# Kernel tuning notes

Measured on AMD Instinct MI355X. Metric: run time of the kernel, lower is better.

The kernel has to match this reference:

```python
import jax, jax.numpy as jnp
import numpy as np

B, T, D = 2, 1024, 1024          # batch, seq, d_model
DI = 2 * D                        # ssm d_inner
N = 16                            # ssm state dim
H, HD = 16, 64                    # heads, head_dim
L = 256                           # MLA latent dim
E, K, F = 8, 2, 2048              # experts, top_k, d_ff
EPS = 1.1920929e-07               # torch RMSNorm default eps (float32 finfo eps)
AUX_COEF = 0.01


def rmsnorm(x, w):
    return x * jax.lax.rsqrt(jnp.mean(x * x, axis=-1, keepdims=True) + EPS) * w


def ternary_quantize(w):
    thresh = 0.5 * jnp.mean(jnp.abs(w))
    return (w > thresh).astype(w.dtype) - (w < -thresh).astype(w.dtype)


def ternary_ste(w):
    # forward uses quantized weights; backward is identity (STE)
    return w + jax.lax.stop_gradient(ternary_quantize(w) - w)


def setup_inputs():
    key = jax.random.key(0)
    ks = jax.random.split(key, 20)
    p = lambda k, s: jax.random.normal(k, s, jnp.float32) * 0.02
    return {
        'x': jax.random.normal(ks[0], (B, T, D), jnp.float32),
        'norm1_w': jnp.ones((D,), jnp.float32),
        'norm2_w': jnp.ones((D,), jnp.float32),
        'ssm_in_w': p(ks[1], (2 * DI, D)),
        'ssm_A_w': p(ks[2], (N, DI)),
        'ssm_B_w': p(ks[3], (N, DI)),
        'ssm_C_w': p(ks[4], (N, DI)),
        'ssm_norm_w': jnp.ones((DI,), jnp.float32),
        'ssm_out_w': p(ks[5], (D, DI)),
        'q_w': p(ks[6], (D, D)),
        'kv_down_w': p(ks[7], (L, D)),
        'k_up_w': p(ks[8], (D, L)),
        'v_up_w': p(ks[9], (D, L)),
        'attn_out_w': p(ks[10], (D, D)),
        'fuse_w': p(ks[11], (D, D)),
        'router_w': p(ks[12], (E, D)),
        'e_gate_w': p(ks[13], (E, F, D)),
        'e_up_w': p(ks[14], (E, F, D)),
        'e_down_w': p(ks[15], (E, D, F)),
        'e_gate_g': jnp.full((E,), 1.0 / np.sqrt(D), jnp.float32),
        'e_up_g': jnp.full((E,), 1.0 / np.sqrt(D), jnp.float32),
        'e_down_g': jnp.full((E,), 1.0 / np.sqrt(F), jnp.float32),
    }


def ssm_branch(h, ssm_in_w, ssm_A_w, ssm_B_w, ssm_C_w, ssm_norm_w, ssm_out_w):
    xz = jnp.einsum('btd,ed->bte', h, ssm_in_w)  # [B,T,2*DI]
    x_in = jax.nn.silu(xz[..., :DI]) * jax.nn.sigmoid(xz[..., DI:])  # [B,T,DI]
    A = -jnp.exp(jnp.clip(jnp.einsum('btd,nd->btn', x_in, ssm_A_w), -5.0, 0.0))
    Bs = jnp.einsum('btd,nd->btn', x_in, ssm_B_w)
    Cs = jnp.einsum('btd,nd->btn', x_in, ssm_C_w)

    def step(state, inp):  # state: [B, DI, N]
        xt, at, bt, ct = inp
        state = state * jnp.exp(at)[:, None, :] + xt[..., None] * bt[:, None, :]
        return state, jnp.sum(state * ct[:, None, :], axis=-1)

    init = jnp.zeros((B, DI, N), jnp.float32)
    xs = (x_in.transpose(1, 0, 2), A.transpose(1, 0, 2), Bs.transpose(1, 0, 2), Cs.transpose(1, 0, 2))
    _, ys = jax.lax.scan(step, init, xs)           # [T,B,DI]
    out = rmsnorm(ys.transpose(1, 0, 2), ssm_norm_w)
    return jnp.einsum('bti,di->btd', out, ssm_out_w)


def mla_attention(h, q_w, kv_down_w, k_up_w, v_up_w, attn_out_w):
    q = jnp.einsum('btd,ed->bte', h, q_w)
    lat = jnp.einsum('btd,ld->btl', h, kv_down_w)
    k = jnp.einsum('btl,dl->btd', lat, k_up_w)
    v = jnp.einsum('btl,dl->btd', lat, v_up_w)
    sh = lambda t: t.reshape(B, T, H, HD).transpose(0, 2, 1, 3)  # [B,H,T,HD]
    q, k, v = sh(q), sh(k), sh(v)
    scores = jnp.einsum('bhqd,bhkd->bhqk', q, k) * (HD ** -0.5)
    attn = jax.nn.softmax(scores, axis=-1)
    out = jnp.einsum('bhqk,bhkd->bhqd', attn, v)
    out = out.transpose(0, 2, 1, 3).reshape(B, T, D)
    return jnp.einsum('btd,ed->bte', out, attn_out_w)


def moe(xf, router_w, e_gate_w, e_up_w, e_down_w, e_gate_g, e_up_g, e_down_g):
    logits = jnp.einsum('td,ed->te', xf, router_w)
    probs = jax.nn.softmax(logits, axis=-1)
    topk_p, topk_i = jax.lax.top_k(probs, K)
    topk_w = topk_p / (jnp.sum(topk_p, axis=-1, keepdims=True) + 1e-09)
    # dense combine weights [tokens, E] (0 for non-selected experts -> same math)
    w_full = jnp.sum(jax.nn.one_hot(topk_i, E, dtype=xf.dtype) * topk_w[..., None], axis=1)
    g = jnp.einsum('td,efd->tef', xf, ternary_ste(e_gate_w)) * e_gate_g[None, :, None]
    u = jnp.einsum('td,efd->tef', xf, ternary_ste(e_up_w)) * e_up_g[None, :, None]
    hh = jax.nn.silu(g) * u
    y = jnp.einsum('tef,edf->ted', hh, ternary_ste(e_down_w)) * e_down_g[None, :, None]
    out = jnp.einsum('ted,te->td', y, w_full)
    mean_probs = jnp.mean(probs, axis=0)
    entropy = -jnp.sum(mean_probs * jnp.log(mean_probs + 1e-09))
    aux = -entropy * AUX_COEF
    return out, aux


def reference(x, norm1_w, norm2_w, ssm_in_w, ssm_A_w, ssm_B_w, ssm_C_w, ssm_norm_w, ssm_out_w,
              q_w, kv_down_w, k_up_w, v_up_w, attn_out_w, fuse_w, router_w,
              e_gate_w, e_up_w, e_down_w, e_gate_g, e_up_g, e_down_g):
    h = rmsnorm(x, norm1_w)
    ssm_out = ssm_branch(h, ssm_in_w, ssm_A_w, ssm_B_w, ssm_C_w, ssm_norm_w, ssm_out_w)
    attn_out = mla_attention(h, q_w, kv_down_w, k_up_w, v_up_w, attn_out_w)
    gate = jax.nn.sigmoid(jnp.einsum('btd,ed->bte', h, fuse_w))  # gated fusion
    x = x + gate * ssm_out + (1.0 - gate) * attn_out
    h2 = rmsnorm(x, norm2_w)
    moe_out, aux = moe(h2.reshape(-1, D), router_w, e_gate_w, e_up_w, e_down_w, e_gate_g, e_up_g, e_down_g)
    x = x + moe_out.reshape(B, T, D)
    return x, aux
```

## Files before the change

### kernel.cpp

```cpp
#include <hip/hip_runtime.h>

constexpr int kB = 2, kT = 1024, kD = 1024, kDI = 2048, kH = 16, kE = 8, kF = 2048;
constexpr int kBT = kB * kT;
constexpr float kEPS = 1.1920929e-07f;

constexpr size_t MF = 1024ull * 1024ull;
constexpr size_t F_H      = 0;
constexpr size_t F_HH     = 0;
constexpr size_t F_XIN    = 2*MF;
constexpr size_t F_EXPA   = 6*MF;
constexpr size_t F_CB     = 6*MF + 32768;
constexpr size_t F_CC     = 6*MF + 65536;
constexpr size_t F_P      = 7*MF;
constexpr size_t F_Q      = 8*MF;
constexpr size_t F_S0     = 9*MF;
constexpr size_t F_YS     = 10*MF;
constexpr size_t F_SSMO   = 14*MF;
constexpr size_t F_ATTNO  = 16*MF;
constexpr size_t F_H2     = 18*MF;
constexpr size_t F_NORMED = 20*MF;
constexpr size_t F_QB     = 20*MF;
constexpr size_t F_KB     = 22*MF;
constexpr size_t F_VB     = 24*MF;
constexpr size_t F_LAT    = 26*MF;
constexpr size_t F_CTX    = 26*MF + MF/2;
constexpr size_t F_FUSE   = 28*MF + MF/2;
constexpr size_t F_XZ     = 31*MF;
constexpr size_t F_SCORES = 31*MF;
constexpr size_t F_QG8    = 31*MF;
constexpr size_t F_QU8    = 35*MF;
constexpr size_t F_QD8    = 39*MF;
constexpr size_t F_MISC   = 47*MF;
constexpr size_t P_PART   = F_MISC;
constexpr size_t P_THRESH = F_MISC + 3072;
constexpr size_t P_PROBS  = F_MISC + 3080;
constexpr size_t I_COUNTS = F_MISC + 3088;
constexpr size_t I_OFFS   = F_MISC + 3096;
constexpr size_t I_CURSOR = F_MISC + 3105;
constexpr size_t I_NTILES = F_MISC + 3113;
constexpr size_t I_TILEE  = F_MISC + 3114;
constexpr size_t I_TILEB  = F_MISC + 3194;
constexpr size_t I_TOPI   = F_MISC + 3274;
constexpr size_t P_TOPW   = F_MISC + 7370;
constexpr size_t I_PAIRT  = F_MISC + 11466;
constexpr size_t P_PAIRW  = F_MISC + 19658;
constexpr size_t WS_FLOATS = F_MISC + 32768;

__device__ __forceinline__ float sigmoidf_(float v) { return 1.f / (1.f + expf(-v)); }

__global__ void zero_k(float* p, int n) {
    int i = blockIdx.x * blockDim.x + threadIdx.x;
    if (i < n) p[i] = 0.f;
}

__global__ __launch_bounds__(256) void rmsnorm_k(const float* __restrict__ x,
                                                 const float* __restrict__ w,
                                                 float* __restrict__ y, int C) {
    int row = blockIdx.x, tid = threadIdx.x;
    const float* xr = x + (size_t)row * C;
    float* yr = y + (size_t)row * C;
    float ss = 0.f;
    for (int c = tid * 4; c < C; c += 1024) {
        float4 v = *(const float4*)(xr + c);
        ss += v.x*v.x + v.y*v.y + v.z*v.z + v.w*v.w;
    }
    for (int off = 32; off; off >>= 1) ss += __shfl_xor(ss, off);
    __shared__ float red[4];
    if ((tid & 63) == 0) red[tid >> 6] = ss;
    __syncthreads();
    ss = red[0] + red[1] + red[2] + red[3];
    float r = rsqrtf(ss / C + kEPS);
    for (int c = tid * 4; c < C; c += 1024) {
        float4 v = *(const float4*)(xr + c);
        float4 g = *(const float4*)(w + c);
        v.x *= r * g.x; v.y *= r * g.y; v.z *= r * g.z; v.w *= r * g.w;
        *(float4*)(yr + c) = v;
    }
}

__global__ __launch_bounds__(256) void gemm_nt(const float* __restrict__ A,
                                               const float* __restrict__ Bm,
                                               float* __restrict__ C,
                                               int K, int lda, int ldb, int ldc,
                                               int bh, long sAb, long sAh, long sBb, long sBh,
                                               long sCb, long sCh) {
    int z = blockIdx.z, zb = z / bh, zh = z - zb * bh;
    A  += (size_t)zb * sAb + (size_t)zh * sAh;
    Bm += (size_t)zb * sBb + (size_t)zh * sBh;
    C  += (size_t)zb * sCb + (size_t)zh * sCh;
    __shared__ __align__(16) float As[16][68], Bs[16][68];
    int tid = threadIdx.x;
    int tx = tid & 15, ty = tid >> 4;
    int m0 = blockIdx.y << 6, n0 = blockIdx.x << 6;
    int lr = tid >> 2, lk = (tid & 3) << 2;
    const float* Ap = A + (size_t)(m0 + lr) * lda + lk;
    const float* Bp = Bm + (size_t)(n0 + lr) * ldb + lk;
    float acc[4][4] = {};
    for (int kt = 0; kt < K; kt += 16) {
        float4 a4 = *(const float4*)(Ap + kt);
        float4 b4 = *(const float4*)(Bp + kt);
        __syncthreads();
        As[lk+0][lr] = a4.x; As[lk+1][lr] = a4.y; As[lk+2][lr] = a4.z; As[lk+3][lr] = a4.w;
        Bs[lk+0][lr] = b4.x; Bs[lk+1][lr] = b4.y; Bs[lk+2][lr] = b4.z; Bs[lk+3][lr] = b4.w;
        __syncthreads();
#pragma unroll
        for (int kk = 0; kk < 16; kk++) {
            float4 av = *(const float4*)&As[kk][ty << 2];
            float4 bv = *(const float4*)&Bs[kk][tx << 2];
            float a_[4] = {av.x, av.y, av.z, av.w};
            float b_[4] = {bv.x, bv.y, bv.z, bv.w};
#pragma unroll
            for (int i = 0; i < 4; i++)
#pragma unroll
                for (int j = 0; j < 4; j++) acc[i][j] = fmaf(a_[i], b_[j], acc[i][j]);
        }
    }
#pragma unroll
    for (int i = 0; i < 4; i++) {
        float4 o = make_float4(acc[i][0], acc[i][1], acc[i][2], acc[i][3]);
        *(float4*)(C + (size_t)(m0 + (ty << 2) + i) * ldc + n0 + (tx << 2)) = o;
    }
}

__global__ __launch_bounds__(256) void gemm_nn(const float* __restrict__ A,
                                               const float* __restrict__ Bm,
                                               float* __restrict__ C,
                                               int K, int lda, int ldb, int ldc,
                                               int bh, long sAb, long sAh, long sBb, long sBh,
                                               long sCb, long sCh) {
    int z = blockIdx.z, zb = z / bh, zh = z - zb * bh;
    A  += (size_t)zb * sAb + (size_t)zh * sAh;
    Bm += (size_t)zb * sBb + (size_t)zh * sBh;
    C  += (size_t)zb * sCb + (size_t)zh * sCh;
    __shared__ __align__(16) float As[16][68], Bs[16][68];
    int tid = threadIdx.x;
    int tx = tid & 15, ty = tid >> 4;
    int m0 = blockIdx.y << 6, n0 = blockIdx.x << 6;
    int lr = tid >> 2, lk = (tid & 3) << 2;
    int bk = tid >> 4, bn = (tid & 15) << 2;
    const float* Ap = A + (size_t)(m0 + lr) * lda + lk;
    const float* Bp = Bm + (size_t)bk * ldb + n0 + bn;
    float acc[4][4] = {};
    for (int kt = 0; kt < K; kt += 16) {
        float4 a4 = *(const float4*)(Ap + kt);
        float4 b4 = *(const float4*)(Bp + (size_t)kt * ldb);
        __syncthreads();
        As[lk+0][lr] = a4.x; As[lk+1][lr] = a4.y; As[lk+2][lr] = a4.z; As[lk+3][lr] = a4.w;
        *(float4*)&Bs[bk][bn] = b4;
        __syncthreads();
#pragma unroll
        for (int kk = 0; kk < 16; kk++) {
            float4 av = *(const float4*)&As[kk][ty << 2];
            float4 bv = *(const float4*)&Bs[kk][tx << 2];
            float a_[4] = {av.x, av.y, av.z, av.w};
            float b_[4] = {bv.x, bv.y, bv.z, bv.w};
#pragma unroll
            for (int i = 0; i < 4; i++)
#pragma unroll
                for (int j = 0; j < 4; j++) acc[i][j] = fmaf(a_[i], b_[j], acc[i][j]);
        }
    }
#pragma unroll
    for (int i = 0; i < 4; i++) {
        float4 o = make_float4(acc[i][0], acc[i][1], acc[i][2], acc[i][3]);
        *(float4*)(C + (size_t)(m0 + (ty << 2) + i) * ldc + n0 + (tx << 2)) = o;
    }
}

__global__ void glu_k(const float* __restrict__ xz, float* __restrict__ xin) {
    int g = blockIdx.x * blockDim.x + threadIdx.x;
    if (g >= kBT * kDI / 4) return;
    int t = g >> 9, c4 = (g & 511) << 2;
    const float* row = xz + (size_t)t * 2 * kDI;
    float4 a = *(const float4*)(row + c4);
    float4 b = *(const float4*)(row + kDI + c4);
    float4 o;
    o.x = a.x * sigmoidf_(a.x) * sigmoidf_(b.x);
    o.y = a.y * sigmoidf_(a.y) * sigmoidf_(b.y);
    o.z = a.z * sigmoidf_(a.z) * sigmoidf_(b.z);
    o.w = a.w * sigmoidf_(a.w) * sigmoidf_(b.w);
    *(float4*)(xin + (size_t)t * kDI + c4) = o;
}

__global__ __launch_bounds__(256) void projabc_k(const float* __restrict__ xin,
                                                 const float* __restrict__ Aw,
                                                 const float* __restrict__ Bw,
                                                 const float* __restrict__ Cw,
                                                 float* __restrict__ expA,
                                                 float* __restrict__ Bc,
                                                 float* __restrict__ Cc) {
    int t = blockIdx.x;
    int wv = threadIdx.x >> 6, lane = threadIdx.x & 63;
    const float* Wp[12];
#pragma unroll
    for (int j = 0; j < 12; j++) {
        int o = wv * 12 + j;
        Wp[j] = (o < 16) ? (Aw + (size_t)o * kDI)
              : (o < 32) ? (Bw + (size_t)(o - 16) * kDI)
                         : (Cw + (size_t)(o - 32) * kDI);
    }
    float part[12] = {};
    const float* xr = xin + (size_t)t * kDI;
    for (int i = 0; i < kDI / 64; i++) {
        int d = lane + (i << 6);
        float xv = xr[d];
#pragma unroll
        for (int j = 0; j < 12; j++) part[j] = fmaf(xv, Wp[j][d], part[j]);
    }
#pragma unroll
    for (int j = 0; j < 12; j++)
        for (int off = 32; off; off >>= 1) part[j] += __shfl_xor(part[j], off);
    if (lane == 0) {
#pragma unroll
        for (int j = 0; j < 12; j++) {
            int o = wv * 12 + j;
            float v = part[j];
            if (o < 16) {
                float zc = fminf(fmaxf(v, -5.f), 0.f);
                expA[(size_t)t * 16 + o] = expf(-expf(zc));
            } else if (o < 32) Bc[(size_t)t * 16 + (o - 16)] = v;
            else Cc[(size_t)t * 16 + (o - 32)] = v;
        }
    }
}

__global__ __launch_bounds__(256) void scan_pass1(const float* __restrict__ xin,
                                                  const float* __restrict__ expA,
                                                  const float* __restrict__ Bc,
                                                  float* __restrict__ Pv, float* __restrict__ Qv) {
    int c = blockIdx.y;
    int ch = blockIdx.x * 256 + threadIdx.x;
    int b = ch >> 11, d = ch & (kDI - 1);
    __shared__ __align__(16) float sE[1024], sB[1024];
    size_t cbase = ((size_t)b * kT + c * 64) * 16;
    *(float4*)(sE + threadIdx.x * 4) = *(const float4*)(expA + cbase + threadIdx.x * 4);
    *(float4*)(sB + threadIdx.x * 4) = *(const float4*)(Bc + cbase + threadIdx.x * 4);
    __syncthreads();
    float s[16], p[16];
#pragma unroll
    for (int n = 0; n < 16; n++) { s[n] = 0.f; p[n] = 1.f; }
    const float* xp = xin + ((size_t)b * kT + c * 64) * kDI + d;
    for (int tl = 0; tl < 64; tl++) {
        float xv = xp[(size_t)tl * kDI];
        const float* e = sE + tl * 16;
        const float* bb = sB + tl * 16;
#pragma unroll
        for (int n = 0; n < 16; n++) {
            float ev = e[n];
            s[n] = s[n] * ev + xv * bb[n];
            p[n] *= ev;
        }
    }
    size_t ob = ((size_t)c * 4096 + ch) * 16;
#pragma unroll
    for (int q = 0; q < 16; q += 4) {
        *(float4*)(Pv + ob + q) = make_float4(p[q], p[q+1], p[q+2], p[q+3]);
        *(float4*)(Qv + ob + q) = make_float4(s[q], s[q+1], s[q+2], s[q+3]);
    }
}

__global__ __launch_bounds__(256) void scan_combine(const float* __restrict__ Pv,
                                                    const float* __restrict__ Qv,
                                                    float* __restrict__ S0) {
    int ch = blockIdx.x * 256 + threadIdx.x;
    float s[16] = {};
    for (int c = 0; c < 16; c++) {
        size_t base = ((size_t)c * 4096 + ch) * 16;
#pragma unroll
        for (int q = 0; q < 16; q += 4)
            *(float4*)(S0 + base + q) = make_float4(s[q], s[q+1], s[q+2], s[q+3]);
#pragma unroll
        for (int q = 0; q < 16; q += 4) {
            float4 pv = *(const float4*)(Pv + base + q);
            float4 qv = *(const float4*)(Qv + base + q);
            s[q+0] = s[q+0] * pv.x + qv.x;
            s[q+1] = s[q+1] * pv.y + qv.y;
            s[q+2] = s[q+2] * pv.z + qv.z;
            s[q+3] = s[q+3] * pv.w + qv.w;
        }
    }
}

__global__ __launch_bounds__(256) void scan_pass2(const float* __restrict__ xin,
                                                  const float* __restrict__ expA,
                                                  const float* __restrict__ Bc,
                                                  const float* __restrict__ Cc,
                                                  const float* __restrict__ S0,
                                                  float* __restrict__ ys) {
    int c = blockIdx.y;
    int ch = blockIdx.x * 256 + threadIdx.x;
    int b = ch >> 11, d = ch & (kDI - 1);
    __shared__ __align__(16) float sE[1024], sB[1024], sC[1024];
    size_t cbase = ((size_t)b * kT + c * 64) * 16;
    *(float4*)(sE + threadIdx.x * 4) = *(const float4*)(expA + cbase + threadIdx.x * 4);
    *(float4*)(sB + threadIdx.x * 4) = *(const float4*)(Bc + cbase + threadIdx.x * 4);
    *(float4*)(sC + threadIdx.x * 4) = *(const float4*)(Cc + cbase + threadIdx.x * 4);
    __syncthreads();
    float s[16];
    size_t sb = ((size_t)c * 4096 + ch) * 16;
#pragma unroll
    for (int q = 0; q < 16; q += 4) {
        float4 v = *(const float4*)(S0 + sb + q);
        s[q] = v.x; s[q+1] = v.y; s[q+2] = v.z; s[q+3] = v.w;
    }
    const float* xp = xin + ((size_t)b * kT + c * 64) * kDI + d;
    float* yp = ys + ((size_t)b * kT + c * 64) * kDI + d;
    for (int tl = 0; tl < 64; tl++) {
        float xv = xp[(size_t)tl * kDI];
        const float* e = sE + tl * 16;
        const float* bb = sB + tl * 16;
        const float* cc = sC + tl * 16;
        float y = 0.f;
#pragma unroll
        for (int n = 0; n < 16; n++) {
            float ev = e[n];
            s[n] = s[n] * ev + xv * bb[n];
            y = fmaf(s[n], cc[n], y);
        }
        yp[(size_t)tl * kDI] = y;
    }
}

__global__ __launch_bounds__(256) void softmax_rows(float* __restrict__ S) {
    size_t row = blockIdx.x;
    float* r = S + row * 1024;
    int tid = threadIdx.x;
    float4 v = *(const float4*)(r + tid * 4);
    v.x *= 0.125f; v.y *= 0.125f; v.z *= 0.125f; v.w *= 0.125f;
    float mx = fmaxf(fmaxf(v.x, v.y), fmaxf(v.z, v.w));
    for (int off = 32; off; off >>= 1) mx = fmaxf(mx, __shfl_xor(mx, off));
    __shared__ float red[4];
    if ((tid & 63) == 0) red[tid >> 6] = mx;
    __syncthreads();
    mx = fmaxf(fmaxf(red[0], red[1]), fmaxf(red[2], red[3]));
    v.x = expf(v.x - mx); v.y = expf(v.y - mx); v.z = expf(v.z - mx); v.w = expf(v.w - mx);
    float sm = v.x + v.y + v.z + v.w;
    for (int off = 32; off; off >>= 1) sm += __shfl_xor(sm, off);
    __syncthreads();
    if ((tid & 63) == 0) red[tid >> 6] = sm;
    __syncthreads();
    sm = red[0] + red[1] + red[2] + red[3];
    float inv = 1.f / sm;
    v.x *= inv; v.y *= inv; v.z *= inv; v.w *= inv;
    *(float4*)(r + tid * 4) = v;
}

__global__ void fuse_k(const float* __restrict__ x, const float* __restrict__ fl,
                       const float* __restrict__ ssm, const float* __restrict__ attn,
                       float* __restrict__ out) {
    int g = blockIdx.x * blockDim.x + threadIdx.x;
    if (g >= kBT * kD / 4) return;
    float4 xv = ((const float4*)x)[g];
    float4 fv = ((const float4*)fl)[g];
    float4 sv = ((const float4*)ssm)[g];
    float4 av = ((const float4*)attn)[g];
    float4 o;
    float gt;
    gt = sigmoidf_(fv.x); o.x = xv.x + gt * sv.x + (1.f - gt) * av.x;
    gt = sigmoidf_(fv.y); o.y = xv.y + gt * sv.y + (1.f - gt) * av.y;
    gt = sigmoidf_(fv.z); o.z = xv.z + gt * sv.z + (1.f - gt) * av.z;
    gt = sigmoidf_(fv.w); o.w = xv.w + gt * sv.w + (1.f - gt) * av.w;
    ((float4*)out)[g] = o;
}

__global__ __launch_bounds__(256) void absmean_partial(const float* __restrict__ w,
                                                       float* __restrict__ part) {
    size_t i0 = ((size_t)blockIdx.x * 256 + threadIdx.x) * 4;
    float s = 0.f;
    for (int it = 0; it < 16; it++) {
        float4 v = *(const float4*)(w + i0 + (size_t)it * 1048576);
        s += fabsf(v.x) + fabsf(v.y) + fabsf(v.z) + fabsf(v.w);
    }
    for (int off = 32; off; off >>= 1) s += __shfl_xor(s, off);
    __shared__ float red[4];
    if ((threadIdx.x & 63) == 0) red[threadIdx.x >> 6] = s;
    __syncthreads();
    if (threadIdx.x == 0) part[blockIdx.x] = red[0] + red[1] + red[2] + red[3];
}

__global__ __launch_bounds__(256) void thresh_k(const float* __restrict__ part,
                                                float* __restrict__ thresh) {
    double s = 0.0;
    for (int i = threadIdx.x; i < 1024; i += 256) s += (double)part[i];
    for (int off = 32; off; off >>= 1) s += __shfl_xor(s, off);
    __shared__ double red[4];
    if ((threadIdx.x & 63) == 0) red[threadIdx.x >> 6] = s;
    __syncthreads();
    if (threadIdx.x == 0) {
        double tot = red[0] + red[1] + red[2] + red[3];
        *thresh = (float)(0.5 * tot / 16777216.0);
    }
}

__global__ void quant_k(const float* __restrict__ w, const float* __restrict__ thresh,
                        signed char* __restrict__ q) {
    float t = *thresh;
    size_t i = ((size_t)blockIdx.x * 256 + threadIdx.x) * 4;
    if (i >= 16777216ull) return;
    float4 v = *(const float4*)(w + i);
    char4 o;
    o.x = (signed char)((v.x > t) - (v.x < -t));
    o.y = (signed char)((v.y > t) - (v.y < -t));
    o.z = (signed char)((v.z > t) - (v.z < -t));
    o.w = (signed char)((v.w > t) - (v.w < -t));
    *(char4*)(q + i) = o;
}

__global__ __launch_bounds__(256) void router_k(const float* __restrict__ h2,
                                                const float* __restrict__ rw,
                                                int* __restrict__ topi, float* __restrict__ topw,
                                                int* __restrict__ counts, float* __restrict__ probsSum) {
    int wv = threadIdx.x >> 6, lane = threadIdx.x & 63;
    int t = blockIdx.x * 4 + wv;
    const float* hr = h2 + (size_t)t * kD;
    float part[8] = {};
    for (int i = 0; i < 16; i++) {
        int d = lane + (i << 6);
        float hv = hr[d];
#pragma unroll
        for (int e = 0; e < 8; e++) part[e] = fmaf(hv, rw[e * kD + d], part[e]);
    }
#pragma unroll
    for (int e = 0; e < 8; e++)
        for (int off = 32; off; off >>= 1) part[e] += __shfl_xor(part[e], off);
    float mx = part[0];
#pragma unroll
    for (int e = 1; e < 8; e++) mx = fmaxf(mx, part[e]);
    float p[8], sum = 0.f;
#pragma unroll
    for (int e = 0; e < 8; e++) { p[e] = expf(part[e] - mx); sum += p[e]; }
    float inv = 1.f / sum;
#pragma unroll
    for (int e = 0; e < 8; e++) p[e] *= inv;
    int i1 = 0; float p1 = p[0];
#pragma unroll
    for (int e = 1; e < 8; e++) if (p[e] > p1) { p1 = p[e]; i1 = e; }
    int i2 = -1; float p2 = -1.f;
#pragma unroll
    for (int e = 0; e < 8; e++) if (e != i1 && p[e] > p2) { p2 = p[e]; i2 = e; }
    if (lane == 0) {
        float wsum = p1 + p2 + 1e-9f;
        topi[2 * t] = i1; topi[2 * t + 1] = i2;
        topw[2 * t] = p1 / wsum; topw[2 * t + 1] = p2 / wsum;
        atomicAdd(&counts[i1], 1); atomicAdd(&counts[i2], 1);
#pragma unroll
        for (int e = 0; e < 8; e++) atomicAdd(&probsSum[e], p[e]);
    }
}

__global__ void route_offsets_k(const int* __restrict__ counts, int* offs, int* cursor,
                                int* pairTok, float* pairW, int* tileE, int* tileB, int* nTiles) {
    if (threadIdx.x != 0 || blockIdx.x != 0) return;
    int off = 0, tc = 0;
    for (int e = 0; e < 8; e++) {
        offs[e] = off; cursor[e] = off;
        int c = counts[e];
        int padded = (c + 63) & ~63;
        for (int p = c; p < padded; p++) { pairTok[off + p] = -1; pairW[off + p] = 0.f; }
        for (int j = 0; j < (padded >> 6); j++) { tileE[tc] = e; tileB[tc] = off + (j << 6); tc++; }
        off += padded;
    }
    offs[8] = off;
    *nTiles = tc;
    for (int j = tc; j < 80; j++) { tileE[j] = 0; tileB[j] = 0; }
}

__global__ void scatter_k(const int* __restrict__ topi, const float* __restrict__ topw,
                          int* cursor, int* pairTok, float* pairW) {
    int t = blockIdx.x * 256 + threadIdx.x;
    if (t >= kBT) return;
    for (int j = 0; j < 2; j++) {
        int e = topi[2 * t + j];
        int pos = atomicAdd(&cursor[e], 1);
        pairTok[pos] = t;
        pairW[pos] = topw[2 * t + j];
    }
}

__global__ __launch_bounds__(256) void moe_gu(const float* __restrict__ h2,
                                              const signed char* __restrict__ qg,
                                              const signed char* __restrict__ qu,
                                              const float* __restrict__ gate_g,
                                              const float* __restrict__ up_g,
                                              const int* __restrict__ tileE, const int* __restrict__ tileB,
                                              const int* __restrict__ nTiles,
                                              const int* __restrict__ pairTok,
                                              float* __restrict__ hh) {
    if ((int)blockIdx.y >= *nTiles) return;
    int te = tileE[blockIdx.y], base = tileB[blockIdx.y];
    __shared__ __align__(16) float As[16][68], Bg[16][68], Bu[16][68];
    __shared__ int sTok[64];
    int tid = threadIdx.x;
    if (tid < 64) sTok[tid] = pairTok[base + tid];
    __syncthreads();
    int tx = tid & 15, ty = tid >> 4;
    int lr = tid >> 2, lk = (tid & 3) << 2;
    int n0 = blockIdx.x << 6;
    int tok = sTok[lr]; if (tok < 0) tok = 0;
    const float* Ap = h2 + (size_t)tok * kD + lk;
    const signed char* Gp = qg + ((size_t)te * kF + n0 + lr) * kD + lk;
    const signed char* Up = qu + ((size_t)te * kF + n0 + lr) * kD + lk;
    float accg[4][4] = {}, accu[4][4] = {};
    for (int kt = 0; kt < kD; kt += 16) {
        float4 a4 = *(const float4*)(Ap + kt);
        char4 g4 = *(const char4*)(Gp + kt);
        char4 u4 = *(const char4*)(Up + kt);
        __syncthreads();
        As[lk+0][lr] = a4.x; As[lk+1][lr] = a4.y; As[lk+2][lr] = a4.z; As[lk+3][lr] = a4.w;
        Bg[lk+0][lr] = (float)g4.x; Bg[lk+1][lr] = (float)g4.y; Bg[lk+2][lr] = (float)g4.z; Bg[lk+3][lr] = (float)g4.w;
        Bu[lk+0][lr] = (float)u4.x; Bu[lk+1][lr] = (float)u4.y; Bu[lk+2][lr] = (float)u4.z; Bu[lk+3][lr] = (float)u4.w;
        __syncthreads();
#pragma unroll
        for (int kk = 0; kk < 16; kk++) {
            float4 av = *(const float4*)&As[kk][ty << 2];
            float4 gv = *(const float4*)&Bg[kk][tx << 2];
            float4 uv = *(const float4*)&Bu[kk][tx << 2];
            float a_[4] = {av.x, av.y, av.z, av.w};
            float g_[4] = {gv.x, gv.y, gv.z, gv.w};
            float u_[4] = {uv.x, uv.y, uv.z, uv.w};
#pragma unroll
            for (int i = 0; i < 4; i++)
#pragma unroll
                for (int j = 0; j < 4; j++) {
                    accg[i][j] = fmaf(a_[i], g_[j], accg[i][j]);
                    accu[i][j] = fmaf(a_[i], u_[j], accu[i][j]);
                }
        }
    }
    float gs = gate_g[te], us = up_g[te];
#pragma unroll
    for (int i = 0; i < 4; i++) {
        float4 o;
        float* op = &o.x;
#pragma unroll
        for (int j = 0; j < 4; j++) {
            float g = accg[i][j] * gs, u = accu[i][j] * us;
            op[j] = g * sigmoidf_(g) * u;
        }
        *(float4*)(hh + (size_t)(base + (ty << 2) + i) * kF + n0 + (tx << 2)) = o;
    }
}

__global__ __launch_bounds__(256) void moe_down(const float* __restrict__ hh,
                                                const signed char* __restrict__ qd,
                                                const float* __restrict__ down_g,
                                                const int* __restrict__ tileE, const int* __restrict__ tileB,
                                                const int* __restrict__ nTiles,
                                                const int* __restrict__ pairTok, const float* __restrict__ pairW,
                                                float* __restrict__ out) {
    if ((int)blockIdx.y >= *nTiles) return;
    int te = tileE[blockIdx.y], base = tileB[blockIdx.y];
    __shared__ __align__(16) float As[16][68], Bs[16][68];
    __shared__ int sTok[64];
    __shared__ float sW[64];
    int tid = threadIdx.x;
    if (tid < 64) { sTok[tid] = pairTok[base + tid]; sW[tid] = pairW[base + tid]; }
    __syncthreads();
    int tx = tid & 15, ty = tid >> 4;
    int lr = tid >> 2, lk = (tid & 3) << 2;
    int n0 = blockIdx.x << 6;
    const float* Ap = hh + (size_t)(base + lr) * kF + lk;
    const signed char* Bp = qd + ((size_t)te * kD + n0 + lr) * kF + lk;
    float acc[4][4] = {};
    for (int kt = 0; kt < kF; kt += 16) {
        float4 a4 = *(const float4*)(Ap + kt);
        char4 b4 = *(const char4*)(Bp + kt);
        __syncthreads();
        As[lk+0][lr] = a4.x; As[lk+1][lr] = a4.y; As[lk+2][lr] = a4.z; As[lk+3][lr] = a4.w;
        Bs[lk+0][lr] = (float)b4.x; Bs[lk+1][lr] = (float)b4.y; Bs[lk+2][lr] = (float)b4.z; Bs[lk+3][lr] = (float)b4.w;
        __syncthreads();
#pragma unroll
        for (int kk = 0; kk < 16; kk++) {
            float4 av = *(const float4*)&As[kk][ty << 2];
            float4 bv = *(const float4*)&Bs[kk][tx << 2];
            float a_[4] = {av.x, av.y, av.z, av.w};
            float b_[4] = {bv.x, bv.y, bv.z, bv.w};
#pragma unroll
            for (int i = 0; i < 4; i++)
#pragma unroll
                for (int j = 0; j < 4; j++) acc[i][j] = fmaf(a_[i], b_[j], acc[i][j]);
        }
    }
    float ds = down_g[te];
#pragma unroll
    for (int i = 0; i < 4; i++) {
        int m = (ty << 2) + i;
        int tok = sTok[m];
        if (tok < 0) continue;
        float wv = sW[m] * ds;
#pragma unroll
        for (int j = 0; j < 4; j++)
            atomicAdd(&out[(size_t)tok * kD + n0 + (tx << 2) + j], acc[i][j] * wv);
    }
}

__global__ void aux_k(const float* __restrict__ probsSum, float* __restrict__ out) {
    if (threadIdx.x != 0 || blockIdx.x != 0) return;
    float ent = 0.f;
    for (int e = 0; e < 8; e++) {
        float p = probsSum[e] * (1.f / (float)kBT);
        ent -= p * logf(p + 1e-9f);
    }
    out[0] = -ent * 0.01f;
}

extern "C" void kernel_launch(void* const* d_in, const int* in_sizes, int n_in,
                              void* d_out, int out_size, void* d_ws, size_t ws_size,
                              hipStream_t stream) {
    const float* x       = (const float*)d_in[0];
    const float* n1w     = (const float*)d_in[1];
    const float* n2w     = (const float*)d_in[2];
    const float* ssm_in_w= (const float*)d_in[3];
    const float* ssm_A_w = (const float*)d_in[4];
    const float* ssm_B_w = (const float*)d_in[5];
    const float* ssm_C_w = (const float*)d_in[6];
    const float* ssm_nw  = (const float*)d_in[7];
    const float* ssm_ow  = (const float*)d_in[8];
    const float* q_w     = (const float*)d_in[9];
    const float* kvd_w   = (const float*)d_in[10];
    const float* kup_w   = (const float*)d_in[11];
    const float* vup_w   = (const float*)d_in[12];
    const float* ao_w    = (const float*)d_in[13];
    const float* fuse_w  = (const float*)d_in[14];
    const float* rtr_w   = (const float*)d_in[15];
    const float* eg_w    = (const float*)d_in[16];
    const float* eu_w    = (const float*)d_in[17];
    const float* ed_w    = (const float*)d_in[18];
    const float* eg_g    = (const float*)d_in[19];
    const float* eu_g    = (const float*)d_in[20];
    const float* ed_g    = (const float*)d_in[21];
    float* out = (float*)d_out;
    float* wsf = (float*)d_ws;
    if (ws_size < WS_FLOATS * sizeof(float)) return;

    float* h      = wsf + F_H;
    float* hh     = wsf + F_HH;
    float* xin    = wsf + F_XIN;
    float* expA   = wsf + F_EXPA;
    float* cB     = wsf + F_CB;
    float* cC     = wsf + F_CC;
    float* Pv     = wsf + F_P;
    float* Qv     = wsf + F_Q;
    float* S0     = wsf + F_S0;
    float* ys     = wsf + F_YS;
    float* ssmo   = wsf + F_SSMO;
    float* attno  = wsf + F_ATTNO;
    float* h2     = wsf + F_H2;
    float* normed = wsf + F_NORMED;
    float* qb     = wsf + F_QB;
    float* kb     = wsf + F_KB;
    float* vb     = wsf + F_VB;
    float* lat    = wsf + F_LAT;
    float* ctx    = wsf + F_CTX;
    float* fuseb  = wsf + F_FUSE;
    float* xz     = wsf + F_XZ;
    float* scores = wsf + F_SCORES;
    signed char* qg = (signed char*)(wsf + F_QG8);
    signed char* qu = (signed char*)(wsf + F_QU8);
    signed char* qd = (signed char*)(wsf + F_QD8);
    float* part   = wsf + P_PART;
    float* thr    = wsf + P_THRESH;
    float* probs  = wsf + P_PROBS;
    int* counts   = (int*)(wsf + I_COUNTS);
    int* offs     = (int*)(wsf + I_OFFS);
    int* cursor   = (int*)(wsf + I_CURSOR);
    int* nTiles   = (int*)(wsf + I_NTILES);
    int* tileE    = (int*)(wsf + I_TILEE);
    int* tileB    = (int*)(wsf + I_TILEB);
    int* topi     = (int*)(wsf + I_TOPI);
    float* topw   = wsf + P_TOPW;
    int* pairT    = (int*)(wsf + I_PAIRT);
    float* pairW  = wsf + P_PAIRW;

    zero_k<<<1, 64, 0, stream>>>(wsf + P_PROBS, 34);
    rmsnorm_k<<<kBT, 256, 0, stream>>>(x, n1w, h, kD);
    gemm_nt<<<dim3(64, 32, 1), 256, 0, stream>>>(h, ssm_in_w, xz, 1024, 1024, 1024, 4096, 1, 0, 0, 0, 0, 0, 0);
    glu_k<<<(kBT * kDI / 4) / 256, 256, 0, stream>>>(xz, xin);
    projabc_k<<<kBT, 256, 0, stream>>>(xin, ssm_A_w, ssm_B_w, ssm_C_w, expA, cB, cC);
    scan_pass1<<<dim3(16, 16, 1), 256, 0, stream>>>(xin, expA, cB, Pv, Qv);
    scan_combine<<<16, 256, 0, stream>>>(Pv, Qv, S0);
    scan_pass2<<<dim3(16, 16, 1), 256, 0, stream>>>(xin, expA, cB, cC, S0, ys);
    rmsnorm_k<<<kBT, 256, 0, stream>>>(ys, ssm_nw, normed, kDI);
    gemm_nt<<<dim3(16, 32, 1), 256, 0, stream>>>(normed, ssm_ow, ssmo, 2048, 2048, 2048, 1024, 1, 0, 0, 0, 0, 0, 0);
    gemm_nt<<<dim3(16, 32, 1), 256, 0, stream>>>(h, q_w, qb, 1024, 1024, 1024, 1024, 1, 0, 0, 0, 0, 0, 0);
    gemm_nt<<<dim3(4, 32, 1), 256, 0, stream>>>(h, kvd_w, lat, 1024, 1024, 1024, 256, 1, 0, 0, 0, 0, 0, 0);
    gemm_nt<<<dim3(16, 32, 1), 256, 0, stream>>>(lat, kup_w, kb, 256, 256, 256, 1024, 1, 0, 0, 0, 0, 0, 0);
    gemm_nt<<<dim3(16, 32, 1), 256, 0, stream>>>(lat, vup_w, vb, 256, 256, 256, 1024, 1, 0, 0, 0, 0, 0, 0);
    for (int b = 0; b < 2; b++) {
        const float* qp = qb + (size_t)b * kT * kD;
        const float* kp = kb + (size_t)b * kT * kD;
        const float* vp = vb + (size_t)b * kT * kD;
        float* ctxp = ctx + (size_t)b * kT * kD;
        gemm_nt<<<dim3(16, 16, 16), 256, 0, stream>>>(qp, kp, scores, 64, 1024, 1024, 1024,
                                                      16, 0, 64, 0, 64, 0, (long)kT * kT);
        softmax_rows<<<kH * kT, 256, 0, stream>>>(scores);
        gemm_nn<<<dim3(1, 16, 16), 256, 0, stream>>>(scores, vp, ctxp, 1024, 1024, 1024, 1024,
                                                     16, 0, (long)kT * kT, 0, 64, 0, 64);
    }
    gemm_nt<<<dim3(16, 32, 1), 256, 0, stream>>>(ctx, ao_w, attno, 1024, 1024, 1024, 1024, 1, 0, 0, 0, 0, 0, 0);
    gemm_nt<<<dim3(16, 32, 1), 256, 0, stream>>>(h, fuse_w, fuseb, 1024, 1024, 1024, 1024, 1, 0, 0, 0, 0, 0, 0);
    fuse_k<<<(kBT * kD / 4) / 256, 256, 0, stream>>>(x, fuseb, ssmo, attno, out);
    rmsnorm_k<<<kBT, 256, 0, stream>>>(out, n2w, h2, kD);
    const float* wsrc[3] = {eg_w, eu_w, ed_w};
    signed char* qdst[3] = {qg, qu, qd};
    for (int i = 0; i < 3; i++) {
        absmean_partial<<<1024, 256, 0, stream>>>(wsrc[i], part + i * 1024);
        thresh_k<<<1, 256, 0, stream>>>(part + i * 1024, thr + i);
        quant_k<<<16384, 256, 0, stream>>>(wsrc[i], thr + i, qdst[i]);
    }
    router_k<<<kBT / 4, 256, 0, stream>>>(h2, rtr_w, topi, topw, counts, probs);
    route_offsets_k<<<1, 64, 0, stream>>>(counts, offs, cursor, pairT, pairW, tileE, tileB, nTiles);
    scatter_k<<<kBT / 256, 256, 0, stream>>>(topi, topw, cursor, pairT, pairW);
    moe_gu<<<dim3(kF / 64, 72, 1), 256, 0, stream>>>(h2, qg, qu, eg_g, eu_g, tileE, tileB, nTiles, pairT, hh);
    moe_down<<<dim3(kD / 64, 72, 1), 256, 0, stream>>>(hh, qd, ed_g, tileE, tileB, nTiles, pairT, pairW, out);
    aux_k<<<1, 64, 0, stream>>>(probs, out + (size_t)kBT * kD);
}
```

Baseline: 2.323 ms.

## Replace FP32 SIMT GEMMs with split-bf16 MFMA GEMMs and bf16 MoE

Swaps all scalar FP32 tiled GEMMs for an MFMA bf16 GEMM. FP32 accuracy is kept by splitting each operand into three bf16 components and concatenating the cross-term products along K (6 segments for dense layers, 3 for attention and latent paths). Attention is restructured into head-group batches with P emitted as split bf16, and the MoE kernels now use bf16 activations and bf16 ternary weights with larger tiles. The workspace layout is reorganized. Many extra split/conversion kernels and much larger effective K are added in exchange for matrix-core throughput, and the 3-term splits trade some precision.

Measured after the change: 4.619 ms. 98.8% more time.

```diff
diff --git a/kernel.cpp b/kernel.cpp
--- a/kernel.cpp
+++ b/kernel.cpp
@@ -4,49 +4,81 @@
 constexpr int kBT = kB * kT;
 constexpr float kEPS = 1.1920929e-07f;
 
-constexpr size_t MF = 1024ull * 1024ull;
-constexpr size_t F_H      = 0;
-constexpr size_t F_HH     = 0;
-constexpr size_t F_XIN    = 2*MF;
-constexpr size_t F_EXPA   = 6*MF;
-constexpr size_t F_CB     = 6*MF + 32768;
-constexpr size_t F_CC     = 6*MF + 65536;
-constexpr size_t F_P      = 7*MF;
-constexpr size_t F_Q      = 8*MF;
-constexpr size_t F_S0     = 9*MF;
-constexpr size_t F_YS     = 10*MF;
-constexpr size_t F_SSMO   = 14*MF;
-constexpr size_t F_ATTNO  = 16*MF;
-constexpr size_t F_H2     = 18*MF;
-constexpr size_t F_NORMED = 20*MF;
-constexpr size_t F_QB     = 20*MF;
-constexpr size_t F_KB     = 22*MF;
-constexpr size_t F_VB     = 24*MF;
-constexpr size_t F_LAT    = 26*MF;
-constexpr size_t F_CTX    = 26*MF + MF/2;
-constexpr size_t F_FUSE   = 28*MF + MF/2;
-constexpr size_t F_XZ     = 31*MF;
-constexpr size_t F_SCORES = 31*MF;
-constexpr size_t F_QG8    = 31*MF;
-constexpr size_t F_QU8    = 35*MF;
-constexpr size_t F_QD8    = 39*MF;
-constexpr size_t F_MISC   = 47*MF;
-constexpr size_t P_PART   = F_MISC;
-constexpr size_t P_THRESH = F_MISC + 3072;
-constexpr size_t P_PROBS  = F_MISC + 3080;
-constexpr size_t I_COUNTS = F_MISC + 3088;
-constexpr size_t I_OFFS   = F_MISC + 3096;
-constexpr size_t I_CURSOR = F_MISC + 3105;
-constexpr size_t I_NTILES = F_MISC + 3113;
-constexpr size_t I_TILEE  = F_MISC + 3114;
-constexpr size_t I_TILEB  = F_MISC + 3194;
-constexpr size_t I_TOPI   = F_MISC + 3274;
-constexpr size_t P_TOPW   = F_MISC + 7370;
-constexpr size_t I_PAIRT  = F_MISC + 11466;
-constexpr size_t P_PAIRW  = F_MISC + 19658;
-constexpr size_t WS_FLOATS = F_MISC + 32768;
-
+typedef unsigned short u16;
+typedef __bf16 bf16x8_t __attribute__((ext_vector_type(8)));
+typedef float f32x4_t __attribute__((ext_vector_type(4)));
+
+__device__ __forceinline__ u16 f2bf(float x) {
+    unsigned int u = __builtin_bit_cast(unsigned int, x);
+    return (u16)((u + 0x7FFFu + ((u >> 16) & 1u)) >> 16);
+}
+__device__ __forceinline__ float bf2f(u16 h) {
+    return __builtin_bit_cast(float, (unsigned int)h << 16);
+}
 __device__ __forceinline__ float sigmoidf_(float v) { return 1.f / (1.f + expf(-v)); }
+
+constexpr int PAT_A6 = (0) | (1 << 3) | (0 << 6) | (1 << 9) | (2 << 12) | (0 << 15);
+constexpr int PAT_B6 = (0) | (0 << 3) | (1 << 6) | (1 << 9) | (0 << 12) | (2 << 15);
+constexpr int PAT_A3 = (0) | (1 << 3) | (0 << 6);
+constexpr int PAT_B3 = (0) | (0 << 3) | (1 << 6);
+
+constexpr size_t MF = 1048576ull;
+constexpr size_t O_HA6   = 0;
+constexpr size_t O_SSMO  = 6*MF;
+constexpr size_t O_ATTNO = 8*MF;
+constexpr size_t O_FUSEB = 10*MF;
+constexpr size_t O_H2F   = 12*MF;
+constexpr size_t O_H2B   = 14*MF;
+constexpr size_t O_LAT   = 15*MF;
+constexpr size_t O_LATA3 = 15*MF + 524288;
+constexpr size_t O_LATB3 = 16*MF + 262144;
+constexpr size_t O_QA3   = 17*MF;
+constexpr size_t O_KB3   = 20*MF;
+constexpr size_t O_VTB3  = 23*MF;
+constexpr size_t O_CTX   = 26*MF;
+constexpr size_t O_WXZ   = 6*MF;
+constexpr size_t O_XZ    = 18*MF;
+constexpr size_t O_XIN   = 6*MF;
+constexpr size_t O_EXPA  = 10*MF;
+constexpr size_t O_CB    = 10*MF + 32768;
+constexpr size_t O_CC    = 10*MF + 65536;
+constexpr size_t O_PV1   = 10*MF + 131072;
+constexpr size_t O_QV1   = 11*MF + 131072;
+constexpr size_t O_S01   = 12*MF + 131072;
+constexpr size_t O_YS    = 13*MF + 262144;
+constexpr size_t O_NORM6 = 28*MF;
+constexpr size_t O_WOUT  = 40*MF;
+constexpr size_t O_WQ    = 28*MF;
+constexpr size_t O_QF    = 29*MF + 524288;
+constexpr size_t O_WKVD  = 31*MF + 524288;
+constexpr size_t O_WKUP  = 31*MF + 917504;
+constexpr size_t O_KF    = 32*MF + 262144;
+constexpr size_t O_WVUP  = 34*MF + 262144;
+constexpr size_t O_VTF   = 34*MF + 655360;
+constexpr size_t O_SCORE = 28*MF;
+constexpr size_t O_P3    = 36*MF;
+constexpr size_t O_CTXA3 = 28*MF;
+constexpr size_t O_WAO   = 31*MF;
+constexpr size_t O_WFUSE = 28*MF;
+constexpr size_t O_QG    = 17*MF;
+constexpr size_t O_QU    = 25*MF;
+constexpr size_t O_QD    = 33*MF;
+constexpr size_t O_HH    = 41*MF;
+constexpr size_t O_MISC  = 48*MF + 262144;
+constexpr size_t M_PROBS = O_MISC + 0;
+constexpr size_t M_COUNT = O_MISC + 8;
+constexpr size_t M_OFFS  = O_MISC + 16;
+constexpr size_t M_CURS  = O_MISC + 25;
+constexpr size_t M_NT    = O_MISC + 33;
+constexpr size_t M_TILEE = O_MISC + 34;
+constexpr size_t M_TILEB = O_MISC + 82;
+constexpr size_t M_TOPI  = O_MISC + 130;
+constexpr size_t M_TOPW  = O_MISC + 4226;
+constexpr size_t M_PAIRT = O_MISC + 8322;
+constexpr size_t M_PAIRW = O_MISC + 16514;
+constexpr size_t M_PART  = O_MISC + 24706;
+constexpr size_t M_THR   = O_MISC + 27778;
+constexpr size_t WS_FLOATS = O_MISC + 32768;
 
 __global__ void zero_k(float* p, int n) {
     int i = blockIdx.x * blockDim.x + threadIdx.x;
@@ -55,10 +87,10 @@
 
 __global__ __launch_bounds__(256) void rmsnorm_k(const float* __restrict__ x,
                                                  const float* __restrict__ w,
-                                                 float* __restrict__ y, int C) {
+                                                 float* __restrict__ yf,
+                                                 u16* __restrict__ yb, int C) {
     int row = blockIdx.x, tid = threadIdx.x;
     const float* xr = x + (size_t)row * C;
-    float* yr = y + (size_t)row * C;
     float ss = 0.f;
     for (int c = tid * 4; c < C; c += 1024) {
         float4 v = *(const float4*)(xr + c);
@@ -74,96 +106,184 @@
         float4 v = *(const float4*)(xr + c);
         float4 g = *(const float4*)(w + c);
         v.x *= r * g.x; v.y *= r * g.y; v.z *= r * g.z; v.w *= r * g.w;
-        *(float4*)(yr + c) = v;
-    }
-}
-
-__global__ __launch_bounds__(256) void gemm_nt(const float* __restrict__ A,
-                                               const float* __restrict__ Bm,
-                                               float* __restrict__ C,
-                                               int K, int lda, int ldb, int ldc,
-                                               int bh, long sAb, long sAh, long sBb, long sBh,
-                                               long sCb, long sCh) {
+        if (yf) *(float4*)(yf + (size_t)row * C + c) = v;
+        if (yb) {
+            ushort4 o; o.x = f2bf(v.x); o.y = f2bf(v.y); o.z = f2bf(v.z); o.w = f2bf(v.w);
+            *(ushort4*)(yb + (size_t)row * C + c) = o;
+        }
+    }
+}
+
+__global__ __launch_bounds__(256) void rmsnorm_splitA6_k(const float* __restrict__ x,
+                                                         const float* __restrict__ w,
+                                                         u16* __restrict__ dst, int C) {
+    int row = blockIdx.x, tid = threadIdx.x;
+    const float* xr = x + (size_t)row * C;
+    float ss = 0.f;
+    for (int c = tid * 4; c < C; c += 1024) {
+        float4 v = *(const float4*)(xr + c);
+        ss += v.x*v.x + v.y*v.y + v.z*v.z + v.w*v.w;
+    }
+    for (int off = 32; off; off >>= 1) ss += __shfl_xor(ss, off);
+    __shared__ float red[4];
+    if ((tid & 63) == 0) red[tid >> 6] = ss;
+    __syncthreads();
+    ss = red[0] + red[1] + red[2] + red[3];
+    float r = rsqrtf(ss / C + kEPS);
+    u16* drow = dst + (size_t)row * 6 * C;
+    for (int c = tid * 4; c < C; c += 1024) {
+        float4 v = *(const float4*)(xr + c);
+        float4 g = *(const float4*)(w + c);
+        float a[4] = {v.x*r*g.x, v.y*r*g.y, v.z*r*g.z, v.w*r*g.w};
+        ushort4 c0, c1, c2;
+        u16* p0 = (u16*)&c0; u16* p1 = (u16*)&c1; u16* p2 = (u16*)&c2;
+#pragma unroll
+        for (int j = 0; j < 4; j++) {
+            float rr = a[j];
+            p0[j] = f2bf(rr); rr -= bf2f(p0[j]);
+            p1[j] = f2bf(rr); rr -= bf2f(p1[j]);
+            p2[j] = f2bf(rr);
+        }
+        *(ushort4*)(drow + 0*C + c) = c0;
+        *(ushort4*)(drow + 1*C + c) = c1;
+        *(ushort4*)(drow + 2*C + c) = c0;
+        *(ushort4*)(drow + 3*C + c) = c1;
+        *(ushort4*)(drow + 4*C + c) = c2;
+        *(ushort4*)(drow + 5*C + c) = c0;
+    }
+}
+
+__global__ __launch_bounds__(256) void split_k(const float* __restrict__ src, u16* __restrict__ dst,
+                                               int lgC, int lgG, int nseg, int pat, int total4) {
+    int i = blockIdx.x * 256 + threadIdx.x;
+    if (i >= total4) return;
+    size_t e = (size_t)i * 4;
+    int C = 1 << lgC;
+    int row = (int)(e >> lgC), col = (int)(e & (C - 1));
+    int g = col >> lgG, cg = col & ((1 << lgG) - 1);
+    float4 v = *(const float4*)(src + e);
+    float a[4] = {v.x, v.y, v.z, v.w};
+    ushort4 comp[3];
+#pragma unroll
+    for (int j = 0; j < 4; j++) {
+        float r = a[j];
+#pragma unroll
+        for (int c = 0; c < 3; c++) {
+            u16 b = f2bf(r);
+            ((u16*)&comp[c])[j] = b;
+            r -= bf2f(b);
+        }
+    }
+    u16* drow = dst + (size_t)row * ((size_t)nseg << lgC) + (((size_t)g * nseg) << lgG) + cg;
+    for (int s = 0; s < nseg; s++) {
+        int c = (pat >> (3 * s)) & 7;
+        *(ushort4*)(drow + ((size_t)s << lgG)) = comp[c];
+    }
+}
+
+template<int WC>
+__global__ __launch_bounds__(256, 2) void mgemm(
+    const u16* __restrict__ A, const u16* __restrict__ B, void* __restrict__ Cp,
+    int K, int lda, int ldb, int ldc, int epi, int bh,
+    long sAb, long sAh, long sBb, long sBh, long sCb, long sCh)
+{
+    constexpr int BM = 128, BN = WC * 64;
+    constexpr int WM = BM / (4 / WC);
+    constexpr int FM = WM / 16;
+    constexpr int ASEG = (BM * 8) / 256;
+    constexpr int BSEG = (BN * 8) / 256;
     int z = blockIdx.z, zb = z / bh, zh = z - zb * bh;
-    A  += (size_t)zb * sAb + (size_t)zh * sAh;
-    Bm += (size_t)zb * sBb + (size_t)zh * sBh;
-    C  += (size_t)zb * sCb + (size_t)zh * sCh;
-    __shared__ __align__(16) float As[16][68], Bs[16][68];
+    const u16* Ab = A + (size_t)zb * sAb + (size_t)zh * sAh;
+    const u16* Bb = B + (size_t)zb * sBb + (size_t)zh * sBh;
+    int m0 = blockIdx.y * BM, n0 = blockIdx.x * BN;
+    __shared__ __align__(16) u16 lsA[BM * 64];
+    __shared__ __align__(16) u16 lsB[BN * 64];
     int tid = threadIdx.x;
-    int tx = tid & 15, ty = tid >> 4;
-    int m0 = blockIdx.y << 6, n0 = blockIdx.x << 6;
-    int lr = tid >> 2, lk = (tid & 3) << 2;
-    const float* Ap = A + (size_t)(m0 + lr) * lda + lk;
-    const float* Bp = Bm + (size_t)(n0 + lr) * ldb + lk;
-    float acc[4][4] = {};
-    for (int kt = 0; kt < K; kt += 16) {
-        float4 a4 = *(const float4*)(Ap + kt);
-        float4 b4 = *(const float4*)(Bp + kt);
+    int w = tid >> 6, l = tid & 63;
+    int wr = w / WC, wc = w % WC;
+    int l15 = l & 15, kg = l >> 4;
+    uint4 ra[ASEG], rb[BSEG];
+
+    auto ld = [&](int kt) {
+#pragma unroll
+        for (int p = 0; p < ASEG; p++) {
+            int s = tid + p * 256, row = s >> 3, kc = s & 7;
+            ra[p] = *(const uint4*)(Ab + (size_t)(m0 + row) * lda + kt * 64 + kc * 8);
+        }
+#pragma unroll
+        for (int p = 0; p < BSEG; p++) {
+            int s = tid + p * 256, row = s >> 3, kc = s & 7;
+            rb[p] = *(const uint4*)(Bb + (size_t)(n0 + row) * ldb + kt * 64 + kc * 8);
+        }
+    };
+    auto st = [&]() {
+#pragma unroll
+        for (int p = 0; p < ASEG; p++) {
+            int s = tid + p * 256, row = s >> 3, kc = s & 7;
+            *(uint4*)(lsA + row * 64 + 8 * (kc ^ (row & 7))) = ra[p];
+        }
+#pragma unroll
+        for (int p = 0; p < BSEG; p++) {
+            int s = tid + p * 256, row = s >> 3, kc = s & 7;
+            *(uint4*)(lsB + row * 64 + 8 * (kc ^ (row & 7))) = rb[p];
+        }
+    };
+
+    f32x4_t acc[FM][4] = {};
+    int nk = K >> 6;
+    ld(0); st(); __syncthreads();
+    for (int kt = 0; kt < nk; kt++) {
+        if (kt + 1 < nk) ld(kt + 1);
+#pragma unroll
+        for (int ks = 0; ks < 2; ks++) {
+            bf16x8_t af[FM], bfv[4];
+            int ke = ks * 32 + kg * 8;
+#pragma unroll
+            for (int m = 0; m < FM; m++) {
+                int r = wr * WM + m * 16 + l15;
+                af[m] = *(const bf16x8_t*)(lsA + r * 64 + (ke ^ ((r & 7) << 3)));
+            }
+#pragma unroll
+            for (int n = 0; n < 4; n++) {
+                int c = wc * 64 + n * 16 + l15;
+                bfv[n] = *(const bf16x8_t*)(lsB + c * 64 + (ke ^ ((c & 7) << 3)));
+            }
+#pragma unroll
+            for (int m = 0; m < FM; m++)
+#pragma unroll
+                for (int n = 0; n < 4; n++)
+                    acc[m][n] = __builtin_amdgcn_mfma_f32_16x16x32_bf16(af[m], bfv[n], acc[m][n], 0, 0, 0);
+        }
         __syncthreads();
-        As[lk+0][lr] = a4.x; As[lk+1][lr] = a4.y; As[lk+2][lr] = a4.z; As[lk+3][lr] = a4.w;
-        Bs[lk+0][lr] = b4.x; Bs[lk+1][lr] = b4.y; Bs[lk+2][lr] = b4.z; Bs[lk+3][lr] = b4.w;
+        if (kt + 1 < nk) st();
         __syncthreads();
-#pragma unroll
-        for (int kk = 0; kk < 16; kk++) {
-            float4 av = *(const float4*)&As[kk][ty << 2];
-            float4 bv = *(const float4*)&Bs[kk][tx << 2];
-            float a_[4] = {av.x, av.y, av.z, av.w};
-            float b_[4] = {bv.x, bv.y, bv.z, bv.w};
-#pragma unroll
-            for (int i = 0; i < 4; i++)
-#pragma unroll
-                for (int j = 0; j < 4; j++) acc[i][j] = fmaf(a_[i], b_[j], acc[i][j]);
-        }
-    }
-#pragma unroll
-    for (int i = 0; i < 4; i++) {
-        float4 o = make_float4(acc[i][0], acc[i][1], acc[i][2], acc[i][3]);
-        *(float4*)(C + (size_t)(m0 + (ty << 2) + i) * ldc + n0 + (tx << 2)) = o;
-    }
-}
-
-__global__ __launch_bounds__(256) void gemm_nn(const float* __restrict__ A,
-                                               const float* __restrict__ Bm,
-                                               float* __restrict__ C,
-                                               int K, int lda, int ldb, int ldc,
-                                               int bh, long sAb, long sAh, long sBb, long sBh,
-                                               long sCb, long sCh) {
-    int z = blockIdx.z, zb = z / bh, zh = z - zb * bh;
-    A  += (size_t)zb * sAb + (size_t)zh * sAh;
-    Bm += (size_t)zb * sBb + (size_t)zh * sBh;
-    C  += (size_t)zb * sCb + (size_t)zh * sCh;
-    __shared__ __align__(16) float As[16][68], Bs[16][68];
-    int tid = threadIdx.x;
-    int tx = tid & 15, ty = tid >> 4;
-    int m0 = blockIdx.y << 6, n0 = blockIdx.x << 6;
-    int lr = tid >> 2, lk = (tid & 3) << 2;
-    int bk = tid >> 4, bn = (tid & 15) << 2;
-    const float* Ap = A + (size_t)(m0 + lr) * lda + lk;
-    const float* Bp = Bm + (size_t)bk * ldb + n0 + bn;
-    float acc[4][4] = {};
-    for (int kt = 0; kt < K; kt += 16) {
-        float4 a4 = *(const float4*)(Ap + kt);
-        float4 b4 = *(const float4*)(Bp + (size_t)kt * ldb);
-        __syncthreads();
-        As[lk+0][lr] = a4.x; As[lk+1][lr] = a4.y; As[lk+2][lr] = a4.z; As[lk+3][lr] = a4.w;
-        *(float4*)&Bs[bk][bn] = b4;
-        __syncthreads();
-#pragma unroll
-        for (int kk = 0; kk < 16; kk++) {
-            float4 av = *(const float4*)&As[kk][ty << 2];
-            float4 bv = *(const float4*)&Bs[kk][tx << 2];
-            float a_[4] = {av.x, av.y, av.z, av.w};
-            float b_[4] = {bv.x, bv.y, bv.z, bv.w};
-#pragma unroll
-            for (int i = 0; i < 4; i++)
-#pragma unroll
-                for (int j = 0; j < 4; j++) acc[i][j] = fmaf(a_[i], b_[j], acc[i][j]);
-        }
-    }
-#pragma unroll
-    for (int i = 0; i < 4; i++) {
-        float4 o = make_float4(acc[i][0], acc[i][1], acc[i][2], acc[i][3]);
-        *(float4*)(C + (size_t)(m0 + (ty << 2) + i) * ldc + n0 + (tx << 2)) = o;
+    }
+    if (epi == 0) {
+        float* C = (float*)Cp + (size_t)zb * sCb + (size_t)zh * sCh;
+#pragma unroll
+        for (int m = 0; m < FM; m++) {
+            int r0 = m0 + wr * WM + m * 16 + kg * 4;
+#pragma unroll
+            for (int n = 0; n < 4; n++) {
+                int c = n0 + wc * 64 + n * 16 + l15;
+#pragma unroll
+                for (int j = 0; j < 4; j++)
+                    C[(size_t)(r0 + j) * ldc + c] = acc[m][n][j];
+            }
+        }
+    } else {
+        u16* C = (u16*)Cp + (size_t)zb * sCb + (size_t)zh * sCh;
+#pragma unroll
+        for (int m = 0; m < FM; m++) {
+            int r0 = m0 + wr * WM + m * 16 + kg * 4;
+#pragma unroll
+            for (int n = 0; n < 4; n++) {
+                int c = n0 + wc * 64 + n * 16 + l15;
+#pragma unroll
+                for (int j = 0; j < 4; j++)
+                    C[(size_t)(r0 + j) * ldc + c] = f2bf(acc[m][n][j]);
+            }
+        }
     }
 }
 
@@ -321,9 +441,10 @@
     }
 }
 
-__global__ __launch_bounds__(256) void softmax_rows(float* __restrict__ S) {
+__global__ __launch_bounds__(256) void softmax_p3(const float* __restrict__ S, u16* __restrict__ P3) {
     size_t row = blockIdx.x;
-    float* r = S + row * 1024;
+    const float* r = S + row * 1024;
+    u16* pr = P3 + row * 3072;
     int tid = threadIdx.x;
     float4 v = *(const float4*)(r + tid * 4);
     v.x *= 0.125f; v.y *= 0.125f; v.z *= 0.125f; v.w *= 0.125f;
@@ -341,8 +462,17 @@
     __syncthreads();
     sm = red[0] + red[1] + red[2] + red[3];
     float inv = 1.f / sm;
-    v.x *= inv; v.y *= inv; v.z *= inv; v.w *= inv;
-    *(float4*)(r + tid * 4) = v;
+    float p[4] = {v.x * inv, v.y * inv, v.z * inv, v.w * inv};
+    ushort4 c0, c1;
+    u16* p0 = (u16*)&c0; u16* p1 = (u16*)&c1;
+#pragma unroll
+    for (int j = 0; j < 4; j++) {
+        p0[j] = f2bf(p[j]);
+        p1[j] = f2bf(p[j] - bf2f(p0[j]));
+    }
+    *(ushort4*)(pr + tid * 4) = c0;
+    *(ushort4*)(pr + 1024 + tid * 4) = c1;
+    *(ushort4*)(pr + 2048 + tid * 4) = c0;
 }
 
 __global__ void fuse_k(const float* __restrict__ x, const float* __restrict__ fl,
@@ -392,18 +522,18 @@
     }
 }
 
-__global__ void quant_k(const float* __restrict__ w, const float* __restrict__ thresh,
-                        signed char* __restrict__ q) {
+__global__ void quantb_k(const float* __restrict__ w, const float* __restrict__ thresh,
+                         u16* __restrict__ q) {
     float t = *thresh;
     size_t i = ((size_t)blockIdx.x * 256 + threadIdx.x) * 4;
     if (i >= 16777216ull) return;
     float4 v = *(const float4*)(w + i);
-    char4 o;
-    o.x = (signed char)((v.x > t) - (v.x < -t));
-    o.y = (signed char)((v.y > t) - (v.y < -t));
-    o.z = (signed char)((v.z > t) - (v.z < -t));
-    o.w = (signed char)((v.w > t) - (v.w < -t));
-    *(char4*)(q + i) = o;
+    ushort4 o;
+    o.x = (v.x > t) ? 0x3F80 : (v.x < -t) ? 0xBF80 : 0;
+    o.y = (v.y > t) ? 0x3F80 : (v.y < -t) ? 0xBF80 : 0;
+    o.z = (v.z > t) ? 0x3F80 : (v.z < -t) ? 0xBF80 : 0;
+    o.w = (v.w > t) ? 0x3F80 : (v.w < -t) ? 0xBF80 : 0;
+    *(ushort4*)(q + i) = o;
 }
 
 __global__ __launch_bounds__(256) void router_k(const float* __restrict__ h2,
@@ -455,14 +585,14 @@
     for (int e = 0; e < 8; e++) {
         offs[e] = off; cursor[e] = off;
         int c = counts[e];
-        int padded = (c + 63) & ~63;
+        int padded = (c + 127) & ~127;
         for (int p = c; p < padded; p++) { pairTok[off + p] = -1; pairW[off + p] = 0.f; }
-        for (int j = 0; j < (padded >> 6); j++) { tileE[tc] = e; tileB[tc] = off + (j << 6); tc++; }
+        for (int j = 0; j < (padded >> 7); j++) { tileE[tc] = e; tileB[tc] = off + (j << 7); tc++; }
         off += padded;
     }
     offs[8] = off;
     *nTiles = tc;
-    for (int j = tc; j < 80; j++) { tileE[j] = 0; tileB[j] = 0; }
+    for (int j = tc; j < 48; j++) { tileE[j] = 0; tileB[j] = 0; }
 }
 
 __global__ void scatter_k(const int* __restrict__ topi, const float* __restrict__ topw,
@@ -477,120 +607,177 @@
     }
 }
 
-__global__ __launch_bounds__(256) void moe_gu(const float* __restrict__ h2,
-                                              const signed char* __restrict__ qg,
-                                              const signed char* __restrict__ qu,
-                                              const float* __restrict__ gate_g,
-                                              const float* __restrict__ up_g,
-                                              const int* __restrict__ tileE, const int* __restrict__ tileB,
-                                              const int* __restrict__ nTiles,
-                                              const int* __restrict__ pairTok,
-                                              float* __restrict__ hh) {
+__global__ __launch_bounds__(256, 2) void moe_gu_m(const u16* __restrict__ h2b,
+    const u16* __restrict__ qg, const u16* __restrict__ qu,
+    const float* __restrict__ gate_g, const float* __restrict__ up_g,
+    const int* __restrict__ tileE, const int* __restrict__ tileB, const int* __restrict__ nTiles,
+    const int* __restrict__ pairTok, u16* __restrict__ hh)
+{
     if ((int)blockIdx.y >= *nTiles) return;
     int te = tileE[blockIdx.y], base = tileB[blockIdx.y];
-    __shared__ __align__(16) float As[16][68], Bg[16][68], Bu[16][68];
-    __shared__ int sTok[64];
+    __shared__ __align__(16) u16 lsA[128 * 64], lsG[64 * 64], lsU[64 * 64];
+    __shared__ int sTok[128];
     int tid = threadIdx.x;
-    if (tid < 64) sTok[tid] = pairTok[base + tid];
-    __syncthreads();
-    int tx = tid & 15, ty = tid >> 4;
-    int lr = tid >> 2, lk = (tid & 3) << 2;
+    if (tid < 128) { int tk = pairTok[base + tid]; sTok[tid] = tk < 0 ? 0 : tk; }
+    __syncthreads();
+    int w = tid >> 6, l = tid & 63, l15 = l & 15, kg = l >> 4;
     int n0 = blockIdx.x << 6;
-    int tok = sTok[lr]; if (tok < 0) tok = 0;
-    const float* Ap = h2 + (size_t)tok * kD + lk;
-    const signed char* Gp = qg + ((size_t)te * kF + n0 + lr) * kD + lk;
-    const signed char* Up = qu + ((size_t)te * kF + n0 + lr) * kD + lk;
-    float accg[4][4] = {}, accu[4][4] = {};
-    for (int kt = 0; kt < kD; kt += 16) {
-        float4 a4 = *(const float4*)(Ap + kt);
-        char4 g4 = *(const char4*)(Gp + kt);
-        char4 u4 = *(const char4*)(Up + kt);
+    const u16* Gb = qg + ((size_t)te * kF + n0) * kD;
+    const u16* Ub = qu + ((size_t)te * kF + n0) * kD;
+    uint4 ra[4], rg[2], ru[2];
+    auto ld = [&](int kt) {
+#pragma unroll
+        for (int p = 0; p < 4; p++) {
+            int s = tid + p * 256, row = s >> 3, kc = s & 7;
+            ra[p] = *(const uint4*)(h2b + (size_t)sTok[row] * kD + kt * 64 + kc * 8);
+        }
+#pragma unroll
+        for (int p = 0; p < 2; p++) {
+            int s = tid + p * 256, row = s >> 3, kc = s & 7;
+            rg[p] = *(const uint4*)(Gb + (size_t)row * kD + kt * 64 + kc * 8);
+            ru[p] = *(const uint4*)(Ub + (size_t)row * kD + kt * 64 + kc * 8);
+        }
+    };
+    auto st = [&]() {
+#pragma unroll
+        for (int p = 0; p < 4; p++) {
+            int s = tid + p * 256, row = s >> 3, kc = s & 7;
+            *(uint4*)(lsA + row * 64 + 8 * (kc ^ (row & 7))) = ra[p];
+        }
+#pragma unroll
+        for (int p = 0; p < 2; p++) {
+            int s = tid + p * 256, row = s >> 3, kc = s & 7;
+            *(uint4*)(lsG + row * 64 + 8 * (kc ^ (row & 7))) = rg[p];
+            *(uint4*)(lsU + row * 64 + 8 * (kc ^ (row & 7))) = ru[p];
+        }
+    };
+    f32x4_t ag[2][4] = {}, au[2][4] = {};
+    ld(0); st(); __syncthreads();
+    for (int kt = 0; kt < 16; kt++) {
+        if (kt + 1 < 16) ld(kt + 1);
+#pragma unroll
+        for (int ks = 0; ks < 2; ks++) {
+            bf16x8_t af[2], gf[4], uf[4];
+            int ke = ks * 32 + kg * 8;
+#pragma unroll
+            for (int m = 0; m < 2; m++) {
+                int r = w * 32 + m * 16 + l15;
+                af[m] = *(const bf16x8_t*)(lsA + r * 64 + (ke ^ ((r & 7) << 3)));
+            }
+#pragma unroll
+            for (int n = 0; n < 4; n++) {
+                int c = n * 16 + l15;
+                gf[n] = *(const bf16x8_t*)(lsG + c * 64 + (ke ^ ((c & 7) << 3)));
+                uf[n] = *(const bf16x8_t*)(lsU + c * 64 + (ke ^ ((c & 7) << 3)));
+            }
+#pragma unroll
+            for (int m = 0; m < 2; m++)
+#pragma unroll
+                for (int n = 0; n < 4; n++) {
+                    ag[m][n] = __builtin_amdgcn_mfma_f32_16x16x32_bf16(af[m], gf[n], ag[m][n], 0, 0, 0);
+                    au[m][n] = __builtin_amdgcn_mfma_f32_16x16x32_bf16(af[m], uf[n], au[m][n], 0, 0, 0);
+                }
+        }
         __syncthreads();
-        As[lk+0][lr] = a4.x; As[lk+1][lr] = a4.y; As[lk+2][lr] = a4.z; As[lk+3][lr] = a4.w;
-        Bg[lk+0][lr] = (float)g4.x; Bg[lk+1][lr] = (float)g4.y; Bg[lk+2][lr] = (float)g4.z; Bg[lk+3][lr] = (float)g4.w;
-        Bu[lk+0][lr] = (float)u4.x; Bu[lk+1][lr] = (float)u4.y; Bu[lk+2][lr] = (float)u4.z; Bu[lk+3][lr] = (float)u4.w;
+        if (kt + 1 < 16) st();
         __syncthreads();
-#pragma unroll
-        for (int kk = 0; kk < 16; kk++) {
-            float4 av = *(const float4*)&As[kk][ty << 2];
-            float4 gv = *(const float4*)&Bg[kk][tx << 2];
-            float4 uv = *(const float4*)&Bu[kk][tx << 2];
-            float a_[4] = {av.x, av.y, av.z, av.w};
-            float g_[4] = {gv.x, gv.y, gv.z, gv.w};
-            float u_[4] = {uv.x, uv.y, uv.z, uv.w};
-#pragma unroll
-            for (int i = 0; i < 4; i++)
-#pragma unroll
-                for (int j = 0; j < 4; j++) {
-                    accg[i][j] = fmaf(a_[i], g_[j], accg[i][j]);
-                    accu[i][j] = fmaf(a_[i], u_[j], accu[i][j]);
-                }
-        }
     }
     float gs = gate_g[te], us = up_g[te];
 #pragma unroll
-    for (int i = 0; i < 4; i++) {
-        float4 o;
-        float* op = &o.x;
-#pragma unroll
-        for (int j = 0; j < 4; j++) {
-            float g = accg[i][j] * gs, u = accu[i][j] * us;
-            op[j] = g * sigmoidf_(g) * u;
-        }
-        *(float4*)(hh + (size_t)(base + (ty << 2) + i) * kF + n0 + (tx << 2)) = o;
-    }
-}
-
-__global__ __launch_bounds__(256) void moe_down(const float* __restrict__ hh,
-                                                const signed char* __restrict__ qd,
-                                                const float* __restrict__ down_g,
-                                                const int* __restrict__ tileE, const int* __restrict__ tileB,
-                                                const int* __restrict__ nTiles,
-                                                const int* __restrict__ pairTok, const float* __restrict__ pairW,
-                                                float* __restrict__ out) {
+    for (int m = 0; m < 2; m++) {
+        int r0 = w * 32 + m * 16 + kg * 4;
+#pragma unroll
+        for (int n = 0; n < 4; n++) {
+            int c = n0 + n * 16 + l15;
+#pragma unroll
+            for (int j = 0; j < 4; j++) {
+                float g = ag[m][n][j] * gs, u = au[m][n][j] * us;
+                float hv = g * sigmoidf_(g) * u;
+                hh[(size_t)(base + r0 + j) * kF + c] = f2bf(hv);
+            }
+        }
+    }
+}
+
+__global__ __launch_bounds__(256, 2) void moe_down_m(const u16* __restrict__ hh,
+    const u16* __restrict__ qd, const float* __restrict__ down_g,
+    const int* __restrict__ tileE, const int* __restrict__ tileB, const int* __restrict__ nTiles,
+    const int* __restrict__ pairTok, const float* __restrict__ pairW,
+    float* __restrict__ out)
+{
     if ((int)blockIdx.y >= *nTiles) return;
     int te = tileE[blockIdx.y], base = tileB[blockIdx.y];
-    __shared__ __align__(16) float As[16][68], Bs[16][68];
-    __shared__ int sTok[64];
-    __shared__ float sW[64];
+    __shared__ __align__(16) u16 lsA[128 * 64], lsB[128 * 64];
+    __shared__ int sTok[128];
+    __shared__ float sW[128];
     int tid = threadIdx.x;
-    if (tid < 64) { sTok[tid] = pairTok[base + tid]; sW[tid] = pairW[base + tid]; }
-    __syncthreads();
-    int tx = tid & 15, ty = tid >> 4;
-    int lr = tid >> 2, lk = (tid & 3) << 2;
-    int n0 = blockIdx.x << 6;
-    const float* Ap = hh + (size_t)(base + lr) * kF + lk;
-    const signed char* Bp = qd + ((size_t)te * kD + n0 + lr) * kF + lk;
-    float acc[4][4] = {};
-    for (int kt = 0; kt < kF; kt += 16) {
-        float4 a4 = *(const float4*)(Ap + kt);
-        char4 b4 = *(const char4*)(Bp + kt);
+    if (tid < 128) { sTok[tid] = pairTok[base + tid]; sW[tid] = pairW[base + tid]; }
+    __syncthreads();
+    int w = tid >> 6, l = tid & 63, l15 = l & 15, kg = l >> 4;
+    int wr = w >> 1, wc = w & 1;
+    int n0 = blockIdx.x << 7;
+    const u16* Ab = hh + (size_t)base * kF;
+    const u16* Bb = qd + ((size_t)te * kD + n0) * kF;
+    uint4 ra[4], rb[4];
+    auto ld = [&](int kt) {
+#pragma unroll
+        for (int p = 0; p < 4; p++) {
+            int s = tid + p * 256, row = s >> 3, kc = s & 7;
+            ra[p] = *(const uint4*)(Ab + (size_t)row * kF + kt * 64 + kc * 8);
+            rb[p] = *(const uint4*)(Bb + (size_t)row * kF + kt * 64 + kc * 8);
+        }
+    };
+    auto st = [&]() {
+#pragma unroll
+        for (int p = 0; p < 4; p++) {
+            int s = tid + p * 256, row = s >> 3, kc = s & 7;
+            *(uint4*)(lsA + row * 64 + 8 * (kc ^ (row & 7))) = ra[p];
+            *(uint4*)(lsB + row * 64 + 8 * (kc ^ (row & 7))) = rb[p];
+        }
+    };
+    f32x4_t acc[4][4] = {};
+    ld(0); st(); __syncthreads();
+    for (int kt = 0; kt < 32; kt++) {
+        if (kt + 1 < 32) ld(kt + 1);
+#pragma unroll
+        for (int ks = 0; ks < 2; ks++) {
+            bf16x8_t af[4], bfv[4];
+            int ke = ks * 32 + kg * 8;
+#pragma unroll
+            for (int m = 0; m < 4; m++) {
+                int r = wr * 64 + m * 16 + l15;
+                af[m] = *(const bf16x8_t*)(lsA + r * 64 + (ke ^ ((r & 7) << 3)));
+            }
+#pragma unroll
+            for (int n = 0; n < 4; n++) {
+                int c = wc * 64 + n * 16 + l15;
+                bfv[n] = *(const bf16x8_t*)(lsB + c * 64 + (ke ^ ((c & 7) << 3)));
+            }
+#pragma unroll
+            for (int m = 0; m < 4; m++)
+#pragma unroll
+                for (int n = 0; n < 4; n++)
+                    acc[m][n] = __builtin_amdgcn_mfma_f32_16x16x32_bf16(af[m], bfv[n], acc[m][n], 0, 0, 0);
+        }
         __syncthreads();
-        As[lk+0][lr] = a4.x; As[lk+1][lr] = a4.y; As[lk+2][lr] = a4.z; As[lk+3][lr] = a4.w;
-        Bs[lk+0][lr] = (float)b4.x; Bs[lk+1][lr] = (float)b4.y; Bs[lk+2][lr] = (float)b4.z; Bs[lk+3][lr] = (float)b4.w;
+        if (kt + 1 < 32) st();
         __syncthreads();
-#pragma unroll
-        for (int kk = 0; kk < 16; kk++) {
-            float4 av = *(const float4*)&As[kk][ty << 2];
-            float4 bv = *(const float4*)&Bs[kk][tx << 2];
-            float a_[4] = {av.x, av.y, av.z, av.w};
-            float b_[4] = {bv.x, bv.y, bv.z, bv.w};
-#pragma unroll
-            for (int i = 0; i < 4; i++)
-#pragma unroll
-                for (int j = 0; j < 4; j++) acc[i][j] = fmaf(a_[i], b_[j], acc[i][j]);
-        }
     }
     float ds = down_g[te];
 #pragma unroll
-    for (int i = 0; i < 4; i++) {
-        int m = (ty << 2) + i;
-        int tok = sTok[m];
-        if (tok < 0) continue;
-        float wv = sW[m] * ds;
-#pragma unroll
-        for (int j = 0; j < 4; j++)
-            atomicAdd(&out[(size_t)tok * kD + n0 + (tx << 2) + j], acc[i][j] * wv);
+    for (int m = 0; m < 4; m++) {
+        int r0 = wr * 64 + m * 16 + kg * 4;
+#pragma unroll
+        for (int n = 0; n < 4; n++) {
+            int c = n0 + wc * 64 + n * 16 + l15;
+#pragma unroll
+            for (int j = 0; j < 4; j++) {
+                int rr = r0 + j;
+                int tok = sTok[rr];
+                if (tok >= 0)
+                    atomicAdd(&out[(size_t)tok * kD + c], acc[m][n][j] * sW[rr] * ds);
+            }
+        }
     }
 }
 
@@ -633,85 +820,114 @@
     float* wsf = (float*)d_ws;
     if (ws_size < WS_FLOATS * sizeof(float)) return;
 
-    float* h      = wsf + F_H;
-    float* hh     = wsf + F_HH;
-    float* xin    = wsf + F_XIN;
-    float* expA   = wsf + F_EXPA;
-    float* cB     = wsf + F_CB;
-    float* cC     = wsf + F_CC;
-    float* Pv     = wsf + F_P;
-    float* Qv     = wsf + F_Q;
-    float* S0     = wsf + F_S0;
-    float* ys     = wsf + F_YS;
-    float* ssmo   = wsf + F_SSMO;
-    float* attno  = wsf + F_ATTNO;
-    float* h2     = wsf + F_H2;
-    float* normed = wsf + F_NORMED;
-    float* qb     = wsf + F_QB;
-    float* kb     = wsf + F_KB;
-    float* vb     = wsf + F_VB;
-    float* lat    = wsf + F_LAT;
-    float* ctx    = wsf + F_CTX;
-    float* fuseb  = wsf + F_FUSE;
-    float* xz     = wsf + F_XZ;
-    float* scores = wsf + F_SCORES;
-    signed char* qg = (signed char*)(wsf + F_QG8);
-    signed char* qu = (signed char*)(wsf + F_QU8);
-    signed char* qd = (signed char*)(wsf + F_QD8);
-    float* part   = wsf + P_PART;
-    float* thr    = wsf + P_THRESH;
-    float* probs  = wsf + P_PROBS;
-    int* counts   = (int*)(wsf + I_COUNTS);
-    int* offs     = (int*)(wsf + I_OFFS);
-    int* cursor   = (int*)(wsf + I_CURSOR);
-    int* nTiles   = (int*)(wsf + I_NTILES);
-    int* tileE    = (int*)(wsf + I_TILEE);
-    int* tileB    = (int*)(wsf + I_TILEB);
-    int* topi     = (int*)(wsf + I_TOPI);
-    float* topw   = wsf + P_TOPW;
-    int* pairT    = (int*)(wsf + I_PAIRT);
-    float* pairW  = wsf + P_PAIRW;
-
-    zero_k<<<1, 64, 0, stream>>>(wsf + P_PROBS, 34);
-    rmsnorm_k<<<kBT, 256, 0, stream>>>(x, n1w, h, kD);
-    gemm_nt<<<dim3(64, 32, 1), 256, 0, stream>>>(h, ssm_in_w, xz, 1024, 1024, 1024, 4096, 1, 0, 0, 0, 0, 0, 0);
+    u16* hA6   = (u16*)(wsf + O_HA6);
+    float* ssmo  = wsf + O_SSMO;
+    float* attno = wsf + O_ATTNO;
+    float* fuseb = wsf + O_FUSEB;
+    float* h2f   = wsf + O_H2F;
+    u16* h2b   = (u16*)(wsf + O_H2B);
+    float* latf  = wsf + O_LAT;
+    u16* latA3 = (u16*)(wsf + O_LATA3);
+    u16* latB3 = (u16*)(wsf + O_LATB3);
+    u16* qA3   = (u16*)(wsf + O_QA3);
+    u16* kB3   = (u16*)(wsf + O_KB3);
+    u16* vtB3  = (u16*)(wsf + O_VTB3);
+    float* ctx   = wsf + O_CTX;
+    u16* wxz   = (u16*)(wsf + O_WXZ);
+    float* xz    = wsf + O_XZ;
+    float* xin   = wsf + O_XIN;
+    float* expA  = wsf + O_EXPA;
+    float* cB    = wsf + O_CB;
+    float* cC    = wsf + O_CC;
+    float* Pv    = wsf + O_PV1;
+    float* Qv    = wsf + O_QV1;
+    float* S0    = wsf + O_S01;
+    float* ys    = wsf + O_YS;
+    u16* norm6 = (u16*)(wsf + O_NORM6);
+    u16* wout  = (u16*)(wsf + O_WOUT);
+    u16* wq    = (u16*)(wsf + O_WQ);
+    float* qf    = wsf + O_QF;
+    u16* wkvd  = (u16*)(wsf + O_WKVD);
+    u16* wkup  = (u16*)(wsf + O_WKUP);
+    float* kf    = wsf + O_KF;
+    u16* wvup  = (u16*)(wsf + O_WVUP);
+    float* vtf   = wsf + O_VTF;
+    float* score = wsf + O_SCORE;
+    u16* P3    = (u16*)(wsf + O_P3);
+    u16* ctxA3 = (u16*)(wsf + O_CTXA3);
+    u16* wao   = (u16*)(wsf + O_WAO);
+    u16* wfuse = (u16*)(wsf + O_WFUSE);
+    u16* qg    = (u16*)(wsf + O_QG);
+    u16* qu    = (u16*)(wsf + O_QU);
+    u16* qd    = (u16*)(wsf + O_QD);
+    u16* hh    = (u16*)(wsf + O_HH);
+    float* probs  = wsf + M_PROBS;
+    int* counts   = (int*)(wsf + M_COUNT);
+    int* offs     = (int*)(wsf + M_OFFS);
+    int* cursor   = (int*)(wsf + M_CURS);
+    int* nTiles   = (int*)(wsf + M_NT);
+    int* tileE    = (int*)(wsf + M_TILEE);
+    int* tileB    = (int*)(wsf + M_TILEB);
+    int* topi     = (int*)(wsf + M_TOPI);
+    float* topw   = wsf + M_TOPW;
+    int* pairT    = (int*)(wsf + M_PAIRT);
+    float* pairW  = wsf + M_PAIRW;
+    float* part   = wsf + M_PART;
+    float* thr    = wsf + M_THR;
+
+    zero_k<<<1, 64, 0, stream>>>(probs, 16);
+    rmsnorm_splitA6_k<<<kBT, 256, 0, stream>>>(x, n1w, hA6, 1024);
+    split_k<<<4096, 256, 0, stream>>>(ssm_in_w, wxz, 10, 10, 6, PAT_B6, 1048576);
+    mgemm<2><<<dim3(32, 16, 1), 256, 0, stream>>>(hA6, wxz, xz, 6144, 6144, 6144, 4096, 0, 1, 0, 0, 0, 0, 0, 0);
     glu_k<<<(kBT * kDI / 4) / 256, 256, 0, stream>>>(xz, xin);
     projabc_k<<<kBT, 256, 0, stream>>>(xin, ssm_A_w, ssm_B_w, ssm_C_w, expA, cB, cC);
     scan_pass1<<<dim3(16, 16, 1), 256, 0, stream>>>(xin, expA, cB, Pv, Qv);
     scan_combine<<<16, 256, 0, stream>>>(Pv, Qv, S0);
     scan_pass2<<<dim3(16, 16, 1), 256, 0, stream>>>(xin, expA, cB, cC, S0, ys);
-    rmsnorm_k<<<kBT, 256, 0, stream>>>(ys, ssm_nw, normed, kDI);
-    gemm_nt<<<dim3(16, 32, 1), 256, 0, stream>>>(normed, ssm_ow, ssmo, 2048, 2048, 2048, 1024, 1, 0, 0, 0, 0, 0, 0);
-    gemm_nt<<<dim3(16, 32, 1), 256, 0, stream>>>(h, q_w, qb, 1024, 1024, 1024, 1024, 1, 0, 0, 0, 0, 0, 0);
-    gemm_nt<<<dim3(4, 32, 1), 256, 0, stream>>>(h, kvd_w, lat, 1024, 1024, 1024, 256, 1, 0, 0, 0, 0, 0, 0);
-    gemm_nt<<<dim3(16, 32, 1), 256, 0, stream>>>(lat, kup_w, kb, 256, 256, 256, 1024, 1, 0, 0, 0, 0, 0, 0);
-    gemm_nt<<<dim3(16, 32, 1), 256, 0, stream>>>(lat, vup_w, vb, 256, 256, 256, 1024, 1, 0, 0, 0, 0, 0, 0);
-    for (int b = 0; b < 2; b++) {
-        const float* qp = qb + (size_t)b * kT * kD;
-        const float* kp = kb + (size_t)b * kT * kD;
-        const float* vp = vb + (size_t)b * kT * kD;
-        float* ctxp = ctx + (size_t)b * kT * kD;
-        gemm_nt<<<dim3(16, 16, 16), 256, 0, stream>>>(qp, kp, scores, 64, 1024, 1024, 1024,
-                                                      16, 0, 64, 0, 64, 0, (long)kT * kT);
-        softmax_rows<<<kH * kT, 256, 0, stream>>>(scores);
-        gemm_nn<<<dim3(1, 16, 16), 256, 0, stream>>>(scores, vp, ctxp, 1024, 1024, 1024, 1024,
-                                                     16, 0, (long)kT * kT, 0, 64, 0, 64);
-    }
-    gemm_nt<<<dim3(16, 32, 1), 256, 0, stream>>>(ctx, ao_w, attno, 1024, 1024, 1024, 1024, 1, 0, 0, 0, 0, 0, 0);
-    gemm_nt<<<dim3(16, 32, 1), 256, 0, stream>>>(h, fuse_w, fuseb, 1024, 1024, 1024, 1024, 1, 0, 0, 0, 0, 0, 0);
+    rmsnorm_splitA6_k<<<kBT, 256, 0, stream>>>(ys, ssm_nw, norm6, 2048);
+    split_k<<<2048, 256, 0, stream>>>(ssm_ow, wout, 11, 11, 6, PAT_B6, 524288);
+    mgemm<2><<<dim3(8, 16, 1), 256, 0, stream>>>(norm6, wout, ssmo, 12288, 12288, 12288, 1024, 0, 1, 0, 0, 0, 0, 0, 0);
+    split_k<<<1024, 256, 0, stream>>>(q_w, wq, 10, 10, 3, PAT_B3, 262144);
+    mgemm<2><<<dim3(8, 16, 1), 256, 0, stream>>>(hA6, wq, qf, 3072, 6144, 3072, 1024, 0, 1, 0, 0, 0, 0, 0, 0);
+    split_k<<<256, 256, 0, stream>>>(kvd_w, wkvd, 10, 10, 3, PAT_B3, 65536);
+    mgemm<2><<<dim3(2, 16, 1), 256, 0, stream>>>(hA6, wkvd, latf, 3072, 6144, 3072, 256, 0, 1, 0, 0, 0, 0, 0, 0);
+    split_k<<<512, 256, 0, stream>>>(latf, latA3, 8, 8, 3, PAT_A3, 131072);
+    split_k<<<512, 256, 0, stream>>>(latf, latB3, 8, 8, 3, PAT_B3, 131072);
+    split_k<<<256, 256, 0, stream>>>(kup_w, wkup, 8, 8, 3, PAT_B3, 65536);
+    mgemm<2><<<dim3(8, 16, 1), 256, 0, stream>>>(latA3, wkup, kf, 768, 768, 768, 1024, 0, 1, 0, 0, 0, 0, 0, 0);
+    split_k<<<256, 256, 0, stream>>>(vup_w, wvup, 8, 8, 3, PAT_A3, 65536);
+    mgemm<2><<<dim3(8, 8, 2), 256, 0, stream>>>(wvup, latB3, vtf, 768, 768, 768, 1024, 0, 1,
+                                                0, 0, 786432, 0, 1048576, 0);
+    split_k<<<2048, 256, 0, stream>>>(qf, qA3, 10, 6, 3, PAT_A3, 524288);
+    split_k<<<2048, 256, 0, stream>>>(kf, kB3, 10, 6, 3, PAT_B3, 524288);
+    split_k<<<2048, 256, 0, stream>>>(vtf, vtB3, 10, 10, 3, PAT_B3, 524288);
+    for (int hg = 0; hg < 4; hg++) {
+        mgemm<2><<<dim3(8, 8, 8), 256, 0, stream>>>(qA3 + hg * 768, kB3 + hg * 768, score,
+                                                    192, 3072, 3072, 1024, 0, 4,
+                                                    3145728, 192, 3145728, 192, 4194304, 1048576);
+        softmax_p3<<<8192, 256, 0, stream>>>(score, P3);
+        mgemm<1><<<dim3(1, 8, 8), 256, 0, stream>>>(P3, vtB3 + (size_t)hg * 786432, ctx + hg * 256,
+                                                    3072, 3072, 3072, 1024, 0, 4,
+                                                    12582912, 3145728, 3145728, 196608, 1048576, 64);
+    }
+    split_k<<<2048, 256, 0, stream>>>(ctx, ctxA3, 10, 10, 3, PAT_A3, 524288);
+    split_k<<<1024, 256, 0, stream>>>(ao_w, wao, 10, 10, 3, PAT_B3, 262144);
+    mgemm<2><<<dim3(8, 16, 1), 256, 0, stream>>>(ctxA3, wao, attno, 3072, 3072, 3072, 1024, 0, 1, 0, 0, 0, 0, 0, 0);
+    split_k<<<1024, 256, 0, stream>>>(fuse_w, wfuse, 10, 10, 6, PAT_B6, 262144);
+    mgemm<2><<<dim3(8, 16, 1), 256, 0, stream>>>(hA6, wfuse, fuseb, 6144, 6144, 6144, 1024, 0, 1, 0, 0, 0, 0, 0, 0);
     fuse_k<<<(kBT * kD / 4) / 256, 256, 0, stream>>>(x, fuseb, ssmo, attno, out);
-    rmsnorm_k<<<kBT, 256, 0, stream>>>(out, n2w, h2, kD);
+    rmsnorm_k<<<kBT, 256, 0, stream>>>(out, n2w, h2f, h2b, kD);
     const float* wsrc[3] = {eg_w, eu_w, ed_w};
-    signed char* qdst[3] = {qg, qu, qd};
+    u16* qdst[3] = {qg, qu, qd};
     for (int i = 0; i < 3; i++) {
         absmean_partial<<<1024, 256, 0, stream>>>(wsrc[i], part + i * 1024);
         thresh_k<<<1, 256, 0, stream>>>(part + i * 1024, thr + i);
-        quant_k<<<16384, 256, 0, stream>>>(wsrc[i], thr + i, qdst[i]);
-    }
-    router_k<<<kBT / 4, 256, 0, stream>>>(h2, rtr_w, topi, topw, counts, probs);
+        quantb_k<<<16384, 256, 0, stream>>>(wsrc[i], thr + i, qdst[i]);
+    }
+    router_k<<<kBT / 4, 256, 0, stream>>>(h2f, rtr_w, topi, topw, counts, probs);
     route_offsets_k<<<1, 64, 0, stream>>>(counts, offs, cursor, pairT, pairW, tileE, tileB, nTiles);
     scatter_k<<<kBT / 256, 256, 0, stream>>>(topi, topw, cursor, pairT, pairW);
-    moe_gu<<<dim3(kF / 64, 72, 1), 256, 0, stream>>>(h2, qg, qu, eg_g, eu_g, tileE, tileB, nTiles, pairT, hh);
-    moe_down<<<dim3(kD / 64, 72, 1), 256, 0, stream>>>(hh, qd, ed_g, tileE, tileB, nTiles, pairT, pairW, out);
+    moe_gu_m<<<dim3(kF / 64, 48, 1), 256, 0, stream>>>(h2b, qg, qu, eg_g, eu_g, tileE, tileB, nTiles, pairT, hh);
+    moe_down_m<<<dim3(kD / 128, 48, 1), 256, 0, stream>>>(hh, qd, ed_g, tileE, tileB, nTiles, pairT, pairW, out);
     aux_k<<<1, 64, 0, stream>>>(probs, out + (size_t)kBT * kD);
 }
```
